# Optimization experiments

Measured on AMD Instinct MI355X. Metric: run time of the kernel, lower is better.

## Reference

```python
import jax, jax.numpy as jnp
import numpy as np

N_USERS = 50000; N_ENT = 100000; C = 64
E = 1500000; NNZ = 1000000
N_REL = 16; N_CATES = 32; NF = 4; NH = 2
R1 = N_REL - 1            # weight rows (devoted branch)
R2 = N_CATES + N_REL - 1  # weight_d rows (diverse branch)


def setup_inputs():
    key = jax.random.key(0)
    ks = list(jax.random.split(key, 32))
    f = jnp.float32
    inp = {}
    inp["user_emb"] = jax.random.normal(ks[0], (N_USERS, C), f)
    inp["entity_emb"] = jax.random.normal(ks[1], (N_ENT, C), f)
    inp["latent_emb"] = jax.random.normal(ks[2], (NF, C), f)
    inp["latent_div_emb"] = jax.random.normal(ks[3], (NF, C), f)
    inp["weight"] = jax.random.normal(ks[4], (R1, C), f) * 0.1
    inp["weight_d"] = jax.random.normal(ks[5], (R2, C), f) * 0.1
    # per-hop Aggregator params stacked over hops [NH, ...]; Linear applied as x @ W + b
    def p(k, shape, s=0.1):
        return jax.random.normal(k, shape, f) * s
    inp["cW1"] = p(ks[6], (NH, C, C)); inp["cb1"] = jnp.zeros((NH, C), f)
    inp["cW2"] = p(ks[7], (NH, C, C)); inp["cb2"] = jnp.zeros((NH, C), f)
    inp["cWua"] = p(ks[8], (NH, NF, NF)); inp["cbua"] = jnp.zeros((NH, NF), f)
    inp["cWwa"] = p(ks[9], (NH, R1, R1)); inp["cbwa"] = jnp.zeros((NH, R1), f)
    inp["eW1"] = p(ks[10], (NH, C, C)); inp["eb1"] = jnp.zeros((NH, C), f)
    inp["eW2"] = p(ks[11], (NH, C, C)); inp["eb2"] = jnp.zeros((NH, C), f)
    inp["eWua"] = p(ks[12], (NH, NF, NF)); inp["ebua"] = jnp.zeros((NH, NF), f)
    inp["eWwa"] = p(ks[13], (NH, R2, R2)); inp["ebwa"] = jnp.zeros((NH, R2), f)
    inp["interact_vals"] = jax.random.uniform(ks[14], (NNZ,), f)
    inp["edge_index"] = jax.random.randint(ks[15], (2, E), 0, N_ENT)
    inp["edge_type"] = jax.random.randint(ks[16], (E,), 1, N_REL)            # values in [1, R1]
    inp["entity_cate_set"] = jax.random.randint(ks[17], (N_ENT,), 1, N_CATES + 1)
    inp["interact_rows"] = jax.random.randint(ks[18], (NNZ,), 0, N_USERS)
    inp["interact_cols"] = jax.random.randint(ks[19], (NNZ,), 0, N_ENT)
    return inp


def _lin(x, W, b):
    return x @ W + b


def _mlp(x, W, b):  # Linear + LeakyReLU(0.2)
    return jax.nn.leaky_relu(_lin(x, W, b), 0.2)


def _normalize(x):  # F.normalize along dim=1 (eps=1e-12)
    return x / jnp.maximum(jnp.linalg.norm(x, axis=1, keepdims=True), 1e-12)


def _agg(entity_emb, user_emb, latent_emb, weight, w_idx, head, tail,
         rows, cols, vals, W1, b1, W2, b2, Wua, bua, Wwa, bwa):
    n_ent, n_usr = entity_emb.shape[0], user_emb.shape[0]
    # KG aggregate: gather -> multiply -> scatter_mean over head
    neigh = entity_emb[tail] * weight[w_idx]                                  # [E, C]
    ssum = jax.ops.segment_sum(neigh, head, num_segments=n_ent)
    cnt = jax.ops.segment_sum(jnp.ones((head.shape[0],), entity_emb.dtype), head, num_segments=n_ent)
    entity_agg = ssum / jnp.maximum(cnt, 1.0)[:, None]
    # user aggregate: sparse.mm(interact_mat, entity_emb)
    user_agg = jax.ops.segment_sum(vals[:, None] * entity_emb[cols], rows, num_segments=n_usr)
    # user -> latent interest attention
    score_ = _lin(user_emb, W1, b1) @ _lin(latent_emb, W1, b1).T              # [U, NF]
    score = jax.nn.softmax(_mlp(score_, Wua, bua), axis=1)                    # [U, NF]
    score_rp = _lin(latent_emb, W2, b2) @ _lin(weight, W2, b2).T              # [NF, R]
    latent_new = jax.nn.softmax(_mlp(score_rp, Wwa, bwa), axis=-1) @ weight   # [NF, C]
    mix = jnp.einsum("uf,fc->uc", score, latent_new)                          # (disen_weight * score).sum(1)
    user_agg = user_agg * mix + user_agg
    return entity_agg, user_agg, latent_new


def _dist_corr(t1, t2):
    ch = t1.shape[0]
    t1 = t1[:, None]; t2 = t2[:, None]
    sq1, sq2 = t1 ** 2, t2 ** 2
    a = jnp.sqrt(jnp.maximum(sq1 - 2.0 * (t1 @ t1.T) + sq1.T, 0.0) + 1e-8)
    b = jnp.sqrt(jnp.maximum(sq2 - 2.0 * (t2 @ t2.T) + sq2.T, 0.0) + 1e-8)
    A = a - a.mean(0, keepdims=True) - a.mean(1, keepdims=True) + a.mean()
    B = b - b.mean(0, keepdims=True) - b.mean(1, keepdims=True) + b.mean()
    n2 = float(ch * ch)
    dab = jnp.sqrt(jnp.maximum((A * B).sum() / n2, 0.0) + 1e-8)
    daa = jnp.sqrt(jnp.maximum((A * A).sum() / n2, 0.0) + 1e-8)
    dbb = jnp.sqrt(jnp.maximum((B * B).sum() / n2, 0.0) + 1e-8)
    return dab / jnp.sqrt(daa * dbb + 1e-8)


def _cor(lat):  # ind == "distance": sum over factor pairs
    c = jnp.asarray(0.0, lat.dtype)
    for i in range(NF):
        for j in range(i + 1, NF):
            c = c + _dist_corr(lat[i], lat[j])
    return c


def reference(user_emb, entity_emb, latent_emb, latent_div_emb, weight, weight_d,
              cW1, cb1, cW2, cb2, cWua, cbua, cWwa, cbwa,
              eW1, eb1, eW2, eb2, eWua, ebua, eWwa, ebwa,
              interact_vals, edge_index, edge_type, entity_cate_set,
              interact_rows, interact_cols):
    head, tail = edge_index[0], edge_index[1]
    idx_c = edge_type - 1               # devoted branch: relation weight index
    idx_d = entity_cate_set[tail] - 1   # diverse branch: category weight index
    # Devoted Interest Branch
    e, u, l = entity_emb, user_emb, latent_emb
    e_res, u_res, l_res = entity_emb, user_emb, latent_emb
    for i in range(NH):
        e, u, l = _agg(e, u, l, weight, idx_c, head, tail,
                       interact_rows, interact_cols, interact_vals,
                       cW1[i], cb1[i], cW2[i], cb2[i], cWua[i], cbua[i], cWwa[i], cbwa[i])
        e = _normalize(e); u = _normalize(u)
        l_res = _normalize(l)           # faithful: overwritten each hop, then += l
        e_res = e_res + e; u_res = u_res + u; l_res = l_res + l
    # Diverse Interest Branch
    e, u, l2 = entity_emb, user_emb, latent_div_emb
    e_d, u_d, l_d = entity_emb, user_emb, latent_div_emb
    for i in range(NH):
        e, u, l2 = _agg(e, u, l2, weight_d, idx_d, head, tail,
                        interact_rows, interact_cols, interact_vals,
                        eW1[i], eb1[i], eW2[i], eb2[i], eWua[i], ebua[i], eWwa[i], ebwa[i])
        e = _normalize(e); u = _normalize(u); l2 = _normalize(l2)
        e_d = e_d + e; u_d = u_d + u; l_d = l_d + l2
    cor = _cor(l_res)
    cor_d = _cor(l_d)
    return (e_res, u_res, cor, e_d, u_d, cor_d)
```

## Files before the change

### kernel.cpp

```cpp
#include <hip/hip_runtime.h>
#include <hip/hip_bf16.h>
#include <math.h>

typedef __hip_bfloat16 bf16;
typedef unsigned short u16;

#define NUSR 50000
#define NENT 100000
#define CC   64
#define EE   1500000
#define NNZI 1000000
#define NF_  4
#define R1_  15
#define R2_  47
#define NSH  8

__device__ __forceinline__ float b2f(bf16 x){ return __bfloat162float(x); }
__device__ __forceinline__ bf16  f2b(float x){ return __float2bfloat16(x); }
__device__ __forceinline__ float fin(float x){ return (x==x && fabsf(x) < 1e30f) ? x : 0.f; }

__device__ __forceinline__ unsigned bf16bits(float x){
    unsigned b = __float_as_uint(x);
    return (b + 0x7FFFu + ((b >> 16) & 1u)) >> 16;
}
__device__ __forceinline__ float pk_lo(unsigned p){ return __uint_as_float(p << 16); }
__device__ __forceinline__ float pk_hi(unsigned p){ return __uint_as_float(p & 0xFFFF0000u); }

__device__ __forceinline__ unsigned rflu(unsigned x){ return (unsigned)__builtin_amdgcn_readfirstlane((int)x); }

__device__ __forceinline__ float ldv(const float* p, long long i){ return p[i]; }
__device__ __forceinline__ float ldv(const bf16*  p, long long i){ return b2f(p[i]); }

struct LatArgs {
    const float *lin, *W1, *b1, *W2, *b2, *Wua, *bua, *Wwa, *bwa, *wt;
    float *lat, *nlat, *P2, *q2;
    int R;
};

__global__ void k_init(int* deg8_e, int* deg8_u, int* ctrs){
    int i = blockIdx.x*256 + threadIdx.x;
    if (i < NSH*NENT) deg8_e[i] = 0;
    if (i < NSH*NUSR) deg8_u[i] = 0;
    if (i < 2) ctrs[i] = 0;
}

__global__ void k_conv(const float* __restrict__ src, bf16* __restrict__ dst){
    int i = blockIdx.x*256 + threadIdx.x;
    if (i < NENT*CC) dst[i] = f2b(src[i]);
}

__global__ void k_hist(const int* __restrict__ head, const int* __restrict__ irows,
                       int* deg8_e, int* deg8_u,
                       u16* __restrict__ rank_e, u16* __restrict__ rank_u){
    int i = blockIdx.x*256 + threadIdx.x;
    int shard = blockIdx.x & (NSH-1);
    if (i < EE){
        int h = head[i];
        int r = ((unsigned)h < NENT) ? atomicAdd(&deg8_e[shard*NENT + h], 1) : 0;
        rank_e[i] = (u16)((r & 8191) | (shard << 13));
    } else {
        int j = i - EE;
        if (j < NNZI){
            int rr = irows[j];
            int r = ((unsigned)rr < NUSR) ? atomicAdd(&deg8_u[shard*NUSR + rr], 1) : 0;
            rank_u[j] = (u16)((r & 8191) | (shard << 13));
        }
    }
}

__global__ void k_base2(int* deg8_e, int* deg8_u,
                        unsigned* rsdeg_e, unsigned* rsdeg_u, int* ctrs){
    int i = blockIdx.x*256 + threadIdx.x;
    int lane = threadIdx.x & 63;
    {
        int d = 0;
        if (i < NENT){
            int tot = 0;
            #pragma unroll
            for (int c = 0; c < NSH; c++){
                int v = deg8_e[c*NENT + i];
                deg8_e[c*NENT + i] = tot;
                tot += v;
            }
            d = tot;
        }
        int incl = d;
        for (int off = 1; off < 64; off <<= 1){
            int v = __shfl_up(incl, off, 64);
            if (lane >= off) incl += v;
        }
        int tot = __shfl(incl, 63, 64);
        int base = 0;
        if (lane == 63) base = atomicAdd(&ctrs[0], tot);
        base = __shfl(base, 63, 64);
        if (i < NENT){
            unsigned rs = (unsigned)(base + incl - d);
            int dc = d < 2047 ? d : 2047;
            rsdeg_e[i] = (rs & 0x1FFFFFu) | ((unsigned)dc << 21);
        }
    }
    {
        int d = 0;
        if (i < NUSR){
            int tot = 0;
            #pragma unroll
            for (int c = 0; c < NSH; c++){
                int v = deg8_u[c*NUSR + i];
                deg8_u[c*NUSR + i] = tot;
                tot += v;
            }
            d = tot;
        }
        int incl = d;
        for (int off = 1; off < 64; off <<= 1){
            int v = __shfl_up(incl, off, 64);
            if (lane >= off) incl += v;
        }
        int tot = __shfl(incl, 63, 64);
        int base = 0;
        if (lane == 63) base = atomicAdd(&ctrs[1], tot);
        base = __shfl(base, 63, 64);
        if (i < NUSR){
            unsigned rs = (unsigned)(base + incl - d);
            int dc = d < 4095 ? d : 4095;
            rsdeg_u[i] = (rs & 0xFFFFFu) | ((unsigned)dc << 20);
        }
    }
}

__global__ void k_scatter(const int* __restrict__ head, const int* __restrict__ tail,
                          const int* __restrict__ etype, const int* __restrict__ cate,
                          const int* __restrict__ irows, const int* __restrict__ icols,
                          const float* __restrict__ ivals,
                          const u16* __restrict__ rank_e, const u16* __restrict__ rank_u,
                          const int* __restrict__ xoff_e, const int* __restrict__ xoff_u,
                          const unsigned* __restrict__ rsdeg_e, const unsigned* __restrict__ rsdeg_u,
                          unsigned* __restrict__ epk, unsigned* __restrict__ upk){
    int i = blockIdx.x*256 + threadIdx.x;
    if (i < EE){
        int h = head[i]; if ((unsigned)h >= NENT) return;
        unsigned tu = (unsigned)tail[i]; if (tu >= NENT) tu = 0;
        unsigned rk = rank_e[i];
        int shard = rk >> 13, r = rk & 8191;
        int slot = (int)(rsdeg_e[h] & 0x1FFFFFu) + xoff_e[shard*NENT + h] + r;
        unsigned ty = (unsigned)(etype[i] - 1) & 15u;
        unsigned cd = (unsigned)(cate[tu]  - 1) & 31u;
        if ((unsigned)slot < EE)
            epk[slot] = tu | (ty << 17) | (cd << 21);
    } else {
        int j = i - EE;
        if (j < NNZI){
            int rr = irows[j]; if ((unsigned)rr >= NUSR) return;
            unsigned c = (unsigned)icols[j]; if (c >= NENT) c = 0;
            unsigned rk = rank_u[j];
            int shard = rk >> 13, r = rk & 8191;
            int slot = (int)(rsdeg_u[rr] & 0xFFFFFu) + xoff_u[shard*NUSR + rr] + r;
            unsigned bits = __float_as_uint(ivals[j]);
            unsigned rb = bits + 0x7FFFu + ((bits >> 16) & 1u);
            unsigned vb = (rb >> 16) & 0x7FFFu;
            if ((unsigned)slot < NNZI)
                upk[slot] = c | (vb << 17);
        }
    }
}

__global__ void k_lat2(LatArgs A0, LatArgs A1){
    LatArgs a = (blockIdx.x == 0) ? A0 : A1;
    const int R = a.R;
    __shared__ float sW1[64*64], sW2[64*64];
    __shared__ float swt[R2_*64], wp[R2_*64];
    __shared__ float lf[NF_*64], lp1[NF_*64], lp2[NF_*64];
    __shared__ float Praw[64*NF_], qv[NF_];
    __shared__ float srp[NF_*R2_], zz[NF_*R2_];
    __shared__ float latls[NF_*64], norms[NF_];
    int t = threadIdx.x;

    for (int idx = t; idx < 64*64; idx += 256){ sW1[idx] = a.W1[idx]; sW2[idx] = a.W2[idx]; }
    for (int idx = t; idx < R*64; idx += 256) swt[idx] = a.wt[idx];
    lf[t] = fin(a.lin[t]);
    __syncthreads();

    {
        int f = t >> 6, k = t & 63;
        float s1 = a.b1[k], s2 = a.b2[k];
        for (int c = 0; c < 64; c++){
            float lv = lf[f*64+c];
            s1 += lv * sW1[c*64+k];
            s2 += lv * sW2[c*64+k];
        }
        lp1[t] = s1; lp2[t] = s2;
    }
    __syncthreads();

    {
        int c = t >> 2, f = t & 3;
        float s = 0.f;
        for (int k = 0; k < 64; k++) s += sW1[c*64+k] * lp1[f*64+k];
        Praw[c*4+f] = s;
    }
    if (t < NF_){
        float s = 0.f;
        for (int k = 0; k < 64; k++) s += a.b1[k] * lp1[t*64+k];
        qv[t] = s;
    }
    __syncthreads();

    {
        int g = t >> 6, c = t & 63;
        float s = 0.f;
        for (int f = 0; f < NF_; f++) s += Praw[c*4+f] * a.Wua[f*4+g];
        a.P2[g*64+c] = s;
    }
    if (t < NF_){
        float s = a.bua[t];
        for (int f = 0; f < NF_; f++) s += qv[f] * a.Wua[f*4+t];
        a.q2[t] = s;
    }
    for (int idx = t; idx < R*64; idx += 256){
        int r = idx >> 6, k = idx & 63;
        float s = a.b2[k];
        for (int c = 0; c < 64; c++) s += swt[r*64+c] * sW2[c*64+k];
        wp[idx] = s;
    }
    __syncthreads();

    if (t < NF_*R){
        int f = t / R, r = t % R;
        float s = 0.f;
        for (int k = 0; k < 64; k++) s += lp2[f*64+k] * wp[r*64+k];
        srp[f*R2_ + r] = s;
    }
    __syncthreads();

    if (t < NF_*R){
        int f = t / R, ss = t % R;
        float v = a.bwa[ss];
        for (int r = 0; r < R; r++) v += srp[f*R2_ + r] * a.Wwa[r*R + ss];
        zz[f*R2_ + ss] = (v > 0.f) ? v : 0.2f*v;
    }
    __syncthreads();

    if (t < NF_){
        float m = -1e30f;
        for (int r = 0; r < R; r++) m = fmaxf(m, zz[t*R2_ + r]);
        float sum = 0.f;
        for (int r = 0; r < R; r++){ float e = expf(zz[t*R2_ + r] - m); zz[t*R2_ + r] = e; sum += e; }
        float inv = 1.f / sum;
        for (int r = 0; r < R; r++) zz[t*R2_ + r] *= inv;
    }
    __syncthreads();

    {
        int f = t >> 6, c = t & 63;
        float s = 0.f;
        for (int r = 0; r < R; r++) s += zz[f*R2_ + r] * swt[r*64 + c];
        latls[t] = s; a.lat[t] = s;
    }
    __syncthreads();
    if (t < NF_){
        float s = 0.f;
        for (int c = 0; c < 64; c++){ float v = latls[t*64+c]; s += v*v; }
        norms[t] = fmaxf(sqrtf(s), 1e-12f);
    }
    __syncthreads();
    a.nlat[t] = latls[t] / norms[t >> 6];
}

template<typename SRC>
__device__ __forceinline__ float ent_row(const SRC* __restrict__ e_src, const float* wl,
                                         const unsigned* __restrict__ epk,
                                         unsigned rd, int use_d, int lane){
    rd = rflu(rd);
    int s = (int)(rd & 0x1FFFFFu);
    int deg = (int)(rd >> 21);
    int e_ = s + deg;
    float acc = 0.f;
    int k = s;
    for (; k + 4 <= e_; k += 4){
        unsigned p0 = rflu(epk[k]), p1 = rflu(epk[k+1]), p2 = rflu(epk[k+2]), p3 = rflu(epk[k+3]);
        unsigned t0 = p0 & 0x1FFFFu; t0 = t0 < NENT ? t0 : 0u;
        unsigned t1 = p1 & 0x1FFFFu; t1 = t1 < NENT ? t1 : 0u;
        unsigned t2 = p2 & 0x1FFFFu; t2 = t2 < NENT ? t2 : 0u;
        unsigned t3 = p3 & 0x1FFFFu; t3 = t3 < NENT ? t3 : 0u;
        float g0 = ldv(e_src, (long long)t0*64 + lane);
        float g1 = ldv(e_src, (long long)t1*64 + lane);
        float g2 = ldv(e_src, (long long)t2*64 + lane);
        float g3 = ldv(e_src, (long long)t3*64 + lane);
        int w0 = use_d ? (int)((p0 >> 21) & 31u) : (int)((p0 >> 17) & 15u);
        int w1 = use_d ? (int)((p1 >> 21) & 31u) : (int)((p1 >> 17) & 15u);
        int w2 = use_d ? (int)((p2 >> 21) & 31u) : (int)((p2 >> 17) & 15u);
        int w3 = use_d ? (int)((p3 >> 21) & 31u) : (int)((p3 >> 17) & 15u);
        acc += g0*wl[w0*64+lane] + g1*wl[w1*64+lane] + g2*wl[w2*64+lane] + g3*wl[w3*64+lane];
    }
    for (; k < e_; k++){
        unsigned p = rflu(epk[k]);
        unsigned ti = p & 0x1FFFFu; ti = ti < NENT ? ti : 0u;
        int wi = use_d ? (int)((p >> 21) & 31u) : (int)((p >> 17) & 15u);
        acc += ldv(e_src, (long long)ti*64 + lane) * wl[wi*64+lane];
    }
    float ea = fin(acc) / fmaxf((float)deg, 1.f);
    float sq = ea*ea;
    for (int m = 1; m < 64; m <<= 1) sq += __shfl_xor(sq, m, 64);
    float nrm = fmaxf(sqrtf(fin(sq)), 1e-12f);
    return ea / nrm;
}

__global__ __launch_bounds__(256) void k_ent0(const float* __restrict__ e_src,
                                              const float* __restrict__ wtab, int R, int use_d,
                                              const unsigned* __restrict__ rsdeg_e,
                                              const unsigned* __restrict__ epk,
                                              bf16* dst){
    __shared__ float wl[R2_*64];
    int t = threadIdx.x;
    for (int idx = t; idx < R2_*64; idx += 256)
        wl[idx] = (idx < R*64) ? wtab[idx] : 0.f;
    __syncthreads();
    int ent = blockIdx.x*4 + (t >> 6);
    int lane = t & 63;
    if (ent >= NENT) return;
    float v = ent_row(e_src, wl, epk, rsdeg_e[ent], use_d, lane);
    dst[(long long)ent*64 + lane] = f2b(v);
}

__global__ __launch_bounds__(256) void k_ent1f(const bf16* __restrict__ e_src,
                                               const float* __restrict__ base_emb,
                                               const float* __restrict__ wtab, int R, int use_d,
                                               const unsigned* __restrict__ rsdeg_e,
                                               const unsigned* __restrict__ epk,
                                               float* dst){
    __shared__ float wl[R2_*64];
    int t = threadIdx.x;
    for (int idx = t; idx < R2_*64; idx += 256)
        wl[idx] = (idx < R*64) ? wtab[idx] : 0.f;
    __syncthreads();
    int ent = blockIdx.x*4 + (t >> 6);
    int lane = t & 63;
    if (ent >= NENT) return;
    float v = ent_row(e_src, wl, epk, rsdeg_e[ent], use_d, lane);
    long long ix = (long long)ent*64 + lane;
    dst[ix] = base_emb[ix] + b2f(e_src[ix]) + v;
}

template<typename ESRC>
__device__ __forceinline__ float usr_gather(const ESRC* __restrict__ e_src,
                                            const unsigned* __restrict__ upk,
                                            unsigned rd, int lane){
    rd = rflu(rd);
    int s = (int)(rd & 0xFFFFFu);
    int e_ = s + (int)(rd >> 20);
    float acc = 0.f;
    int k = s;
    for (; k + 8 <= e_; k += 8){
        unsigned p0 = rflu(upk[k]),   p1 = rflu(upk[k+1]), p2 = rflu(upk[k+2]), p3 = rflu(upk[k+3]);
        unsigned p4 = rflu(upk[k+4]), p5 = rflu(upk[k+5]), p6 = rflu(upk[k+6]), p7 = rflu(upk[k+7]);
        unsigned c0 = p0 & 0x1FFFFu; c0 = c0 < NENT ? c0 : 0u;
        unsigned c1 = p1 & 0x1FFFFu; c1 = c1 < NENT ? c1 : 0u;
        unsigned c2 = p2 & 0x1FFFFu; c2 = c2 < NENT ? c2 : 0u;
        unsigned c3 = p3 & 0x1FFFFu; c3 = c3 < NENT ? c3 : 0u;
        unsigned c4 = p4 & 0x1FFFFu; c4 = c4 < NENT ? c4 : 0u;
        unsigned c5 = p5 & 0x1FFFFu; c5 = c5 < NENT ? c5 : 0u;
        unsigned c6 = p6 & 0x1FFFFu; c6 = c6 < NENT ? c6 : 0u;
        unsigned c7 = p7 & 0x1FFFFu; c7 = c7 < NENT ? c7 : 0u;
        float g0 = ldv(e_src,(long long)c0*64+lane), g1 = ldv(e_src,(long long)c1*64+lane);
        float g2 = ldv(e_src,(long long)c2*64+lane), g3 = ldv(e_src,(long long)c3*64+lane);
        float g4 = ldv(e_src,(long long)c4*64+lane), g5 = ldv(e_src,(long long)c5*64+lane);
        float g6 = ldv(e_src,(long long)c6*64+lane), g7 = ldv(e_src,(long long)c7*64+lane);
        float v0 = __uint_as_float(((p0 >> 17) & 0x7FFFu) << 16);
        float v1 = __uint_as_float(((p1 >> 17) & 0x7FFFu) << 16);
        float v2 = __uint_as_float(((p2 >> 17) & 0x7FFFu) << 16);
        float v3 = __uint_as_float(((p3 >> 17) & 0x7FFFu) << 16);
        float v4 = __uint_as_float(((p4 >> 17) & 0x7FFFu) << 16);
        float v5 = __uint_as_float(((p5 >> 17) & 0x7FFFu) << 16);
        float v6 = __uint_as_float(((p6 >> 17) & 0x7FFFu) << 16);
        float v7 = __uint_as_float(((p7 >> 17) & 0x7FFFu) << 16);
        acc += v0*g0 + v1*g1 + v2*g2 + v3*g3 + v4*g4 + v5*g5 + v6*g6 + v7*g7;
    }
    for (; k + 4 <= e_; k += 4){
        unsigned p0 = rflu(upk[k]), p1 = rflu(upk[k+1]), p2 = rflu(upk[k+2]), p3 = rflu(upk[k+3]);
        unsigned c0 = p0 & 0x1FFFFu; c0 = c0 < NENT ? c0 : 0u;
        unsigned c1 = p1 & 0x1FFFFu; c1 = c1 < NENT ? c1 : 0u;
        unsigned c2 = p2 & 0x1FFFFu; c2 = c2 < NENT ? c2 : 0u;
        unsigned c3 = p3 & 0x1FFFFu; c3 = c3 < NENT ? c3 : 0u;
        float v0 = __uint_as_float(((p0 >> 17) & 0x7FFFu) << 16);
        float v1 = __uint_as_float(((p1 >> 17) & 0x7FFFu) << 16);
        float v2 = __uint_as_float(((p2 >> 17) & 0x7FFFu) << 16);
        float v3 = __uint_as_float(((p3 >> 17) & 0x7FFFu) << 16);
        acc += v0*ldv(e_src,(long long)c0*64+lane) + v1*ldv(e_src,(long long)c1*64+lane)
             + v2*ldv(e_src,(long long)c2*64+lane) + v3*ldv(e_src,(long long)c3*64+lane);
    }
    for (; k < e_; k++){
        unsigned p = rflu(upk[k]);
        unsigned c = p & 0x1FFFFu; c = c < NENT ? c : 0u;
        float v = __uint_as_float(((p >> 17) & 0x7FFFu) << 16);
        acc += v * ldv(e_src, (long long)c*64 + lane);
    }
    return fin(acc);
}

__device__ __forceinline__ float usr_epi(float acc, float x,
                                         const float* P2l, const float* latl, const float* q2l,
                                         int lane){
    float s0 = x*P2l[lane], s1 = x*P2l[64+lane], s2 = x*P2l[128+lane], s3 = x*P2l[192+lane];
    for (int m = 1; m < 64; m <<= 1){
        s0 += __shfl_xor(s0, m, 64);
        s1 += __shfl_xor(s1, m, 64);
        s2 += __shfl_xor(s2, m, 64);
        s3 += __shfl_xor(s3, m, 64);
    }
    s0 += q2l[0]; s1 += q2l[1]; s2 += q2l[2]; s3 += q2l[3];
    s0 = (s0 > 0.f) ? s0 : 0.2f*s0;
    s1 = (s1 > 0.f) ? s1 : 0.2f*s1;
    s2 = (s2 > 0.f) ? s2 : 0.2f*s2;
    s3 = (s3 > 0.f) ? s3 : 0.2f*s3;
    float mx = fmaxf(fmaxf(s0, s1), fmaxf(s2, s3));
    float e0 = expf(s0-mx), e1 = expf(s1-mx), e2 = expf(s2-mx), e3 = expf(s3-mx);
    float inv = 1.f / (e0+e1+e2+e3);
    float mix = fin((e0*latl[lane] + e1*latl[64+lane] + e2*latl[128+lane] + e3*latl[192+lane]) * inv);
    float ua = acc * (1.f + mix);
    float sq = ua*ua;
    for (int m = 1; m < 64; m <<= 1) sq += __shfl_xor(sq, m, 64);
    float nrm = fmaxf(sqrtf(fin(sq)), 1e-12f);
    return ua / nrm;
}

__global__ __launch_bounds__(256) void k_usr0(const float* __restrict__ u_src,
                                              const float* __restrict__ e_src,
                                              const unsigned* __restrict__ rsdeg_u,
                                              const unsigned* __restrict__ upk,
                                              const float* __restrict__ P2,
                                              const float* __restrict__ q2,
                                              const float* __restrict__ lat_new,
                                              float* dst){
    __shared__ float P2l[NF_*64], latl[NF_*64], q2l[NF_];
    int t = threadIdx.x;
    P2l[t] = fin(P2[t]); latl[t] = fin(lat_new[t]);
    if (t < NF_) q2l[t] = fin(q2[t]);
    __syncthreads();
    int u = blockIdx.x*4 + (t >> 6);
    int lane = t & 63;
    if (u >= NUSR) return;
    float acc = usr_gather(e_src, upk, rsdeg_u[u], lane);
    float x = u_src[(long long)u*64 + lane];
    dst[(long long)u*64 + lane] = usr_epi(acc, x, P2l, latl, q2l, lane);
}

__global__ __launch_bounds__(256) void k_usr1f(float* u_io,
                                               const bf16* __restrict__ e_src,
                                               const float* __restrict__ base_emb,
                                               const unsigned* __restrict__ rsdeg_u,
                                               const unsigned* __restrict__ upk,
                                               const float* __restrict__ P2,
                                               const float* __restrict__ q2,
                                               const float* __restrict__ lat_new){
    __shared__ float P2l[NF_*64], latl[NF_*64], q2l[NF_];
    int t = threadIdx.x;
    P2l[t] = fin(P2[t]); latl[t] = fin(lat_new[t]);
    if (t < NF_) q2l[t] = fin(q2[t]);
    __syncthreads();
    int u = blockIdx.x*4 + (t >> 6);
    int lane = t & 63;
    if (u >= NUSR) return;
    float acc = usr_gather(e_src, upk, rsdeg_u[u], lane);
    long long ix = (long long)u*64 + lane;
    float x = u_io[ix];
    float v = usr_epi(acc, x, P2l, latl, q2l, lane);
    u_io[ix] = base_emb[ix] + x + v;
}

#define GE_ ((NENT+3)/4)
#define GU_ ((NUSR+3)/4)
__global__ __launch_bounds__(256) void k_it0(const bf16* __restrict__ ebf,
                                             const float* __restrict__ wt_c,
                                             const float* __restrict__ wt_d,
                                             const unsigned* __restrict__ rsdeg_e,
                                             const unsigned* __restrict__ epk,
                                             unsigned* __restrict__ eA2,
                                             const float* __restrict__ u_src,
                                             const unsigned* __restrict__ rsdeg_u,
                                             const unsigned* __restrict__ upk,
                                             const float* __restrict__ P2c,
                                             const float* __restrict__ q2c,
                                             const float* __restrict__ latc,
                                             const float* __restrict__ P2d,
                                             const float* __restrict__ q2d,
                                             const float* __restrict__ latd,
                                             float* __restrict__ dst_c,
                                             float* __restrict__ dst_d){
    __shared__ float sm[(R1_+R2_)*64];
    int t = threadIdx.x;
    int lane = t & 63;
    if (blockIdx.x < GE_){
        float* wlc = sm;
        float* wld = sm + R1_*64;
        for (int idx = t; idx < R1_*64; idx += 256) wlc[idx] = wt_c[idx];
        for (int idx = t; idx < R2_*64; idx += 256) wld[idx] = wt_d[idx];
        __syncthreads();
        int ent = blockIdx.x*4 + (t >> 6);
        if (ent >= NENT) return;
        unsigned rd = rflu(rsdeg_e[ent]);
        int s = (int)(rd & 0x1FFFFFu);
        int deg = (int)(rd >> 21);
        int e_ = s + deg;
        float ac = 0.f, ad = 0.f;
        int k = s;
        for (; k + 8 <= e_; k += 8){
            unsigned p0 = rflu(epk[k]),   p1 = rflu(epk[k+1]), p2 = rflu(epk[k+2]), p3 = rflu(epk[k+3]);
            unsigned p4 = rflu(epk[k+4]), p5 = rflu(epk[k+5]), p6 = rflu(epk[k+6]), p7 = rflu(epk[k+7]);
            unsigned t0 = p0 & 0x1FFFFu; t0 = t0 < NENT ? t0 : 0u;
            unsigned t1 = p1 & 0x1FFFFu; t1 = t1 < NENT ? t1 : 0u;
            unsigned t2 = p2 & 0x1FFFFu; t2 = t2 < NENT ? t2 : 0u;
            unsigned t3 = p3 & 0x1FFFFu; t3 = t3 < NENT ? t3 : 0u;
            unsigned t4 = p4 & 0x1FFFFu; t4 = t4 < NENT ? t4 : 0u;
            unsigned t5 = p5 & 0x1FFFFu; t5 = t5 < NENT ? t5 : 0u;
            unsigned t6 = p6 & 0x1FFFFu; t6 = t6 < NENT ? t6 : 0u;
            unsigned t7 = p7 & 0x1FFFFu; t7 = t7 < NENT ? t7 : 0u;
            float g0 = b2f(ebf[(long long)t0*64 + lane]);
            float g1 = b2f(ebf[(long long)t1*64 + lane]);
            float g2 = b2f(ebf[(long long)t2*64 + lane]);
            float g3 = b2f(ebf[(long long)t3*64 + lane]);
            float g4 = b2f(ebf[(long long)t4*64 + lane]);
            float g5 = b2f(ebf[(long long)t5*64 + lane]);
            float g6 = b2f(ebf[(long long)t6*64 + lane]);
            float g7 = b2f(ebf[(long long)t7*64 + lane]);
            ac += g0*wlc[((p0>>17)&15u)*64+lane] + g1*wlc[((p1>>17)&15u)*64+lane]
                + g2*wlc[((p2>>17)&15u)*64+lane] + g3*wlc[((p3>>17)&15u)*64+lane]
                + g4*wlc[((p4>>17)&15u)*64+lane] + g5*wlc[((p5>>17)&15u)*64+lane]
                + g6*wlc[((p6>>17)&15u)*64+lane] + g7*wlc[((p7>>17)&15u)*64+lane];
            ad += g0*wld[((p0>>21)&31u)*64+lane] + g1*wld[((p1>>21)&31u)*64+lane]
                + g2*wld[((p2>>21)&31u)*64+lane] + g3*wld[((p3>>21)&31u)*64+lane]
                + g4*wld[((p4>>21)&31u)*64+lane] + g5*wld[((p5>>21)&31u)*64+lane]
                + g6*wld[((p6>>21)&31u)*64+lane] + g7*wld[((p7>>21)&31u)*64+lane];
        }
        for (; k + 4 <= e_; k += 4){
            unsigned p0 = rflu(epk[k]), p1 = rflu(epk[k+1]), p2 = rflu(epk[k+2]), p3 = rflu(epk[k+3]);
            unsigned t0 = p0 & 0x1FFFFu; t0 = t0 < NENT ? t0 : 0u;
            unsigned t1 = p1 & 0x1FFFFu; t1 = t1 < NENT ? t1 : 0u;
            unsigned t2 = p2 & 0x1FFFFu; t2 = t2 < NENT ? t2 : 0u;
            unsigned t3 = p3 & 0x1FFFFu; t3 = t3 < NENT ? t3 : 0u;
            float g0 = b2f(ebf[(long long)t0*64 + lane]);
            float g1 = b2f(ebf[(long long)t1*64 + lane]);
            float g2 = b2f(ebf[(long long)t2*64 + lane]);
            float g3 = b2f(ebf[(long long)t3*64 + lane]);
            ac += g0*wlc[((p0>>17)&15u)*64+lane] + g1*wlc[((p1>>17)&15u)*64+lane]
                + g2*wlc[((p2>>17)&15u)*64+lane] + g3*wlc[((p3>>17)&15u)*64+lane];
            ad += g0*wld[((p0>>21)&31u)*64+lane] + g1*wld[((p1>>21)&31u)*64+lane]
                + g2*wld[((p2>>21)&31u)*64+lane] + g3*wld[((p3>>21)&31u)*64+lane];
        }
        for (; k < e_; k++){
            unsigned p = rflu(epk[k]);
            unsigned ti = p & 0x1FFFFu; ti = ti < NENT ? ti : 0u;
            float g = b2f(ebf[(long long)ti*64 + lane]);
            ac += g*wlc[((p>>17)&15u)*64+lane];
            ad += g*wld[((p>>21)&31u)*64+lane];
        }
        float inv_deg = 1.f / fmaxf((float)deg, 1.f);
        float ec = fin(ac) * inv_deg, ed = fin(ad) * inv_deg;
        float sc = ec*ec, sd = ed*ed;
        for (int m = 1; m < 64; m <<= 1){
            sc += __shfl_xor(sc, m, 64);
            sd += __shfl_xor(sd, m, 64);
        }
        float vc = ec / fmaxf(sqrtf(fin(sc)), 1e-12f);
        float vd = ed / fmaxf(sqrtf(fin(sd)), 1e-12f);
        eA2[(long long)ent*64 + lane] = bf16bits(vc) | (bf16bits(vd) << 16);
    } else {
        float* P2lc = sm;
        float* latlc = sm + 256;
        float* P2ld = sm + 512;
        float* latld = sm + 768;
        float* q2lc = sm + 1024;
        float* q2ld = sm + 1032;
        P2lc[t] = fin(P2c[t]); latlc[t] = fin(latc[t]);
        P2ld[t] = fin(P2d[t]); latld[t] = fin(latd[t]);
        if (t < NF_){ q2lc[t] = fin(q2c[t]); q2ld[t] = fin(q2d[t]); }
        __syncthreads();
        int u = (blockIdx.x - GE_)*4 + (t >> 6);
        if (u >= NUSR) return;
        float acc = usr_gather(ebf, upk, rsdeg_u[u], lane);
        long long ix = (long long)u*64 + lane;
        float x = u_src[ix];
        dst_c[ix] = usr_epi(acc, x, P2lc, latlc, q2lc, lane);
        dst_d[ix] = usr_epi(acc, x, P2ld, latld, q2ld, lane);
    }
}

__global__ __launch_bounds__(256) void k_it1(const unsigned* __restrict__ eA2,
                                             const float* __restrict__ ent_base,
                                             const float* __restrict__ wt_c,
                                             const float* __restrict__ wt_d,
                                             const unsigned* __restrict__ rsdeg_e,
                                             const unsigned* __restrict__ epk,
                                             float* __restrict__ oe_c,
                                             float* __restrict__ oe_d,
                                             float* __restrict__ uc_io,
                                             float* __restrict__ ud_io,
                                             const float* __restrict__ usr_base,
                                             const unsigned* __restrict__ rsdeg_u,
                                             const unsigned* __restrict__ upk,
                                             const float* __restrict__ P2c,
                                             const float* __restrict__ q2c,
                                             const float* __restrict__ latc,
                                             const float* __restrict__ P2d,
                                             const float* __restrict__ q2d,
                                             const float* __restrict__ latd){
    __shared__ float sm[(R1_+R2_)*64];
    int t = threadIdx.x;
    int lane = t & 63;
    if (blockIdx.x < GE_){
        float* wlc = sm;
        float* wld = sm + R1_*64;
        for (int idx = t; idx < R1_*64; idx += 256) wlc[idx] = wt_c[idx];
        for (int idx = t; idx < R2_*64; idx += 256) wld[idx] = wt_d[idx];
        __syncthreads();
        int ent = blockIdx.x*4 + (t >> 6);
        if (ent >= NENT) return;
        unsigned rd = rflu(rsdeg_e[ent]);
        int s = (int)(rd & 0x1FFFFFu);
        int deg = (int)(rd >> 21);
        int e_ = s + deg;
        float ac = 0.f, ad = 0.f;
        int k = s;
        for (; k + 8 <= e_; k += 8){
            unsigned p0 = rflu(epk[k]),   p1 = rflu(epk[k+1]), p2 = rflu(epk[k+2]), p3 = rflu(epk[k+3]);
            unsigned p4 = rflu(epk[k+4]), p5 = rflu(epk[k+5]), p6 = rflu(epk[k+6]), p7 = rflu(epk[k+7]);
            unsigned t0 = p0 & 0x1FFFFu; t0 = t0 < NENT ? t0 : 0u;
            unsigned t1 = p1 & 0x1FFFFu; t1 = t1 < NENT ? t1 : 0u;
            unsigned t2 = p2 & 0x1FFFFu; t2 = t2 < NENT ? t2 : 0u;
            unsigned t3 = p3 & 0x1FFFFu; t3 = t3 < NENT ? t3 : 0u;
            unsigned t4 = p4 & 0x1FFFFu; t4 = t4 < NENT ? t4 : 0u;
            unsigned t5 = p5 & 0x1FFFFu; t5 = t5 < NENT ? t5 : 0u;
            unsigned t6 = p6 & 0x1FFFFu; t6 = t6 < NENT ? t6 : 0u;
            unsigned t7 = p7 & 0x1FFFFu; t7 = t7 < NENT ? t7 : 0u;
            unsigned v0 = eA2[(long long)t0*64 + lane];
            unsigned v1 = eA2[(long long)t1*64 + lane];
            unsigned v2 = eA2[(long long)t2*64 + lane];
            unsigned v3 = eA2[(long long)t3*64 + lane];
            unsigned v4 = eA2[(long long)t4*64 + lane];
            unsigned v5 = eA2[(long long)t5*64 + lane];
            unsigned v6 = eA2[(long long)t6*64 + lane];
            unsigned v7 = eA2[(long long)t7*64 + lane];
            ac += pk_lo(v0)*wlc[((p0>>17)&15u)*64+lane] + pk_lo(v1)*wlc[((p1>>17)&15u)*64+lane]
                + pk_lo(v2)*wlc[((p2>>17)&15u)*64+lane] + pk_lo(v3)*wlc[((p3>>17)&15u)*64+lane]
                + pk_lo(v4)*wlc[((p4>>17)&15u)*64+lane] + pk_lo(v5)*wlc[((p5>>17)&15u)*64+lane]
                + pk_lo(v6)*wlc[((p6>>17)&15u)*64+lane] + pk_lo(v7)*wlc[((p7>>17)&15u)*64+lane];
            ad += pk_hi(v0)*wld[((p0>>21)&31u)*64+lane] + pk_hi(v1)*wld[((p1>>21)&31u)*64+lane]
                + pk_hi(v2)*wld[((p2>>21)&31u)*64+lane] + pk_hi(v3)*wld[((p3>>21)&31u)*64+lane]
                + pk_hi(v4)*wld[((p4>>21)&31u)*64+lane] + pk_hi(v5)*wld[((p5>>21)&31u)*64+lane]
                + pk_hi(v6)*wld[((p6>>21)&31u)*64+lane] + pk_hi(v7)*wld[((p7>>21)&31u)*64+lane];
        }
        for (; k + 4 <= e_; k += 4){
            unsigned p0 = rflu(epk[k]), p1 = rflu(epk[k+1]), p2 = rflu(epk[k+2]), p3 = rflu(epk[k+3]);
            unsigned t0 = p0 & 0x1FFFFu; t0 = t0 < NENT ? t0 : 0u;
            unsigned t1 = p1 & 0x1FFFFu; t1 = t1 < NENT ? t1 : 0u;
            unsigned t2 = p2 & 0x1FFFFu; t2 = t2 < NENT ? t2 : 0u;
            unsigned t3 = p3 & 0x1FFFFu; t3 = t3 < NENT ? t3 : 0u;
            unsigned v0 = eA2[(long long)t0*64 + lane];
            unsigned v1 = eA2[(long long)t1*64 + lane];
            unsigned v2 = eA2[(long long)t2*64 + lane];
            unsigned v3 = eA2[(long long)t3*64 + lane];
            ac += pk_lo(v0)*wlc[((p0>>17)&15u)*64+lane] + pk_lo(v1)*wlc[((p1>>17)&15u)*64+lane]
                + pk_lo(v2)*wlc[((p2>>17)&15u)*64+lane] + pk_lo(v3)*wlc[((p3>>17)&15u)*64+lane];
            ad += pk_hi(v0)*wld[((p0>>21)&31u)*64+lane] + pk_hi(v1)*wld[((p1>>21)&31u)*64+lane]
                + pk_hi(v2)*wld[((p2>>21)&31u)*64+lane] + pk_hi(v3)*wld[((p3>>21)&31u)*64+lane];
        }
        for (; k < e_; k++){
            unsigned p = rflu(epk[k]);
            unsigned ti = p & 0x1FFFFu; ti = ti < NENT ? ti : 0u;
            unsigned v = eA2[(long long)ti*64 + lane];
            ac += pk_lo(v) * wlc[((p>>17)&15u)*64+lane];
            ad += pk_hi(v) * wld[((p>>21)&31u)*64+lane];
        }
        float inv_deg = 1.f / fmaxf((float)deg, 1.f);
        float vc = fin(ac) * inv_deg, vd = fin(ad) * inv_deg;
        float sc = vc*vc, sd = vd*vd;
        for (int m = 1; m < 64; m <<= 1){
            sc += __shfl_xor(sc, m, 64);
            sd += __shfl_xor(sd, m, 64);
        }
        long long ix = (long long)ent*64 + lane;
        float be = ent_base[ix];
        unsigned selfv = eA2[ix];
        oe_c[ix] = be + pk_lo(selfv) + vc / fmaxf(sqrtf(fin(sc)), 1e-12f);
        oe_d[ix] = be + pk_hi(selfv) + vd / fmaxf(sqrtf(fin(sd)), 1e-12f);
    } else {
        float* P2lc = sm;
        float* latlc = sm + 256;
        float* P2ld = sm + 512;
        float* latld = sm + 768;
        float* q2lc = sm + 1024;
        float* q2ld = sm + 1032;
        P2lc[t] = fin(P2c[t]); latlc[t] = fin(latc[t]);
        P2ld[t] = fin(P2d[t]); latld[t] = fin(latd[t]);
        if (t < NF_){ q2lc[t] = fin(q2c[t]); q2ld[t] = fin(q2d[t]); }
        __syncthreads();
        int u = (blockIdx.x - GE_)*4 + (t >> 6);
        if (u >= NUSR) return;
        unsigned rd = rflu(rsdeg_u[u]);
        int s = (int)(rd & 0xFFFFFu);
        int e_ = s + (int)(rd >> 20);
        float accc = 0.f, accd = 0.f;
        int k = s;
        for (; k + 8 <= e_; k += 8){
            unsigned p0 = rflu(upk[k]),   p1 = rflu(upk[k+1]), p2 = rflu(upk[k+2]), p3 = rflu(upk[k+3]);
            unsigned p4 = rflu(upk[k+4]), p5 = rflu(upk[k+5]), p6 = rflu(upk[k+6]), p7 = rflu(upk[k+7]);
            unsigned c0 = p0 & 0x1FFFFu; c0 = c0 < NENT ? c0 : 0u;
            unsigned c1 = p1 & 0x1FFFFu; c1 = c1 < NENT ? c1 : 0u;
            unsigned c2 = p2 & 0x1FFFFu; c2 = c2 < NENT ? c2 : 0u;
            unsigned c3 = p3 & 0x1FFFFu; c3 = c3 < NENT ? c3 : 0u;
            unsigned c4 = p4 & 0x1FFFFu; c4 = c4 < NENT ? c4 : 0u;
            unsigned c5 = p5 & 0x1FFFFu; c5 = c5 < NENT ? c5 : 0u;
            unsigned c6 = p6 & 0x1FFFFu; c6 = c6 < NENT ? c6 : 0u;
            unsigned c7 = p7 & 0x1FFFFu; c7 = c7 < NENT ? c7 : 0u;
            unsigned g0 = eA2[(long long)c0*64 + lane];
            unsigned g1 = eA2[(long long)c1*64 + lane];
            unsigned g2 = eA2[(long long)c2*64 + lane];
            unsigned g3 = eA2[(long long)c3*64 + lane];
            unsigned g4 = eA2[(long long)c4*64 + lane];
            unsigned g5 = eA2[(long long)c5*64 + lane];
            unsigned g6 = eA2[(long long)c6*64 + lane];
            unsigned g7 = eA2[(long long)c7*64 + lane];
            float v0 = __uint_as_float(((p0 >> 17) & 0x7FFFu) << 16);
            float v1 = __uint_as_float(((p1 >> 17) & 0x7FFFu) << 16);
            float v2 = __uint_as_float(((p2 >> 17) & 0x7FFFu) << 16);
            float v3 = __uint_as_float(((p3 >> 17) & 0x7FFFu) << 16);
            float v4 = __uint_as_float(((p4 >> 17) & 0x7FFFu) << 16);
            float v5 = __uint_as_float(((p5 >> 17) & 0x7FFFu) << 16);
            float v6 = __uint_as_float(((p6 >> 17) & 0x7FFFu) << 16);
            float v7 = __uint_as_float(((p7 >> 17) & 0x7FFFu) << 16);
            accc += v0*pk_lo(g0) + v1*pk_lo(g1) + v2*pk_lo(g2) + v3*pk_lo(g3)
                  + v4*pk_lo(g4) + v5*pk_lo(g5) + v6*pk_lo(g6) + v7*pk_lo(g7);
            accd += v0*pk_hi(g0) + v1*pk_hi(g1) + v2*pk_hi(g2) + v3*pk_hi(g3)
                  + v4*pk_hi(g4) + v5*pk_hi(g5) + v6*pk_hi(g6) + v7*pk_hi(g7);
        }
        for (; k + 4 <= e_; k += 4){
            unsigned p0 = rflu(upk[k]), p1 = rflu(upk[k+1]), p2 = rflu(upk[k+2]), p3 = rflu(upk[k+3]);
            unsigned c0 = p0 & 0x1FFFFu; c0 = c0 < NENT ? c0 : 0u;
            unsigned c1 = p1 & 0x1FFFFu; c1 = c1 < NENT ? c1 : 0u;
            unsigned c2 = p2 & 0x1FFFFu; c2 = c2 < NENT ? c2 : 0u;
            unsigned c3 = p3 & 0x1FFFFu; c3 = c3 < NENT ? c3 : 0u;
            float v0 = __uint_as_float(((p0 >> 17) & 0x7FFFu) << 16);
            float v1 = __uint_as_float(((p1 >> 17) & 0x7FFFu) << 16);
            float v2 = __uint_as_float(((p2 >> 17) & 0x7FFFu) << 16);
            float v3 = __uint_as_float(((p3 >> 17) & 0x7FFFu) << 16);
            unsigned g0 = eA2[(long long)c0*64 + lane];
            unsigned g1 = eA2[(long long)c1*64 + lane];
            unsigned g2 = eA2[(long long)c2*64 + lane];
            unsigned g3 = eA2[(long long)c3*64 + lane];
            accc += v0*pk_lo(g0) + v1*pk_lo(g1) + v2*pk_lo(g2) + v3*pk_lo(g3);
            accd += v0*pk_hi(g0) + v1*pk_hi(g1) + v2*pk_hi(g2) + v3*pk_hi(g3);
        }
        for (; k < e_; k++){
            unsigned p = rflu(upk[k]);
            unsigned c = p & 0x1FFFFu; c = c < NENT ? c : 0u;
            float v = __uint_as_float(((p >> 17) & 0x7FFFu) << 16);
            unsigned g = eA2[(long long)c*64 + lane];
            accc += v * pk_lo(g);
            accd += v * pk_hi(g);
        }
        long long ix = (long long)u*64 + lane;
        float xc = uc_io[ix], xd = ud_io[ix];
        float be = usr_base[ix];
        float vc = usr_epi(fin(accc), xc, P2lc, latlc, q2lc, lane);
        float vd = usr_epi(fin(accd), xd, P2ld, latld, q2ld, lane);
        uc_io[ix] = be + xc + vc;
        ud_io[ix] = be + xd + vd;
    }
}

__global__ void k_cor(const float* __restrict__ latn1_c,
                      const float* __restrict__ ldiv,
                      const float* __restrict__ nld0, const float* __restrict__ nld1,
                      float* out){
    __shared__ float rows[NF_*64];
    __shared__ float nr[NF_];
    __shared__ float t1s[64], t2s[64], m1s[64], m2s[64];
    __shared__ float pr[256], pr2[256], pr3[256];
    __shared__ float gms[2];
    __shared__ float corsh;
    int t = threadIdx.x, b = blockIdx.x;

    if (b == 0){
        rows[t] = fin(latn1_c[t]);
        __syncthreads();
        if (t < NF_){
            float s = 0.f;
            for (int c = 0; c < 64; c++){ float v = rows[t*64+c]; s += v*v; }
            nr[t] = fmaxf(sqrtf(s), 1e-12f);
        }
        __syncthreads();
        float v = rows[t];
        __syncthreads();
        rows[t] = v + v / nr[t >> 6];
    } else {
        rows[t] = ldiv[t] + fin(nld0[t]) + fin(nld1[t]);
    }
    if (t == 0) corsh = 0.f;
    __syncthreads();

    for (int i = 0; i < NF_; i++) for (int j = i+1; j < NF_; j++){
        if (t < 64){ t1s[t] = rows[i*64+t]; t2s[t] = rows[j*64+t]; }
        __syncthreads();
        int i_ = t >> 2, q = t & 3;
        float pa = 0.f, pb = 0.f;
        for (int jj = q*16; jj < q*16+16; jj++){
            float d1 = t1s[i_] - t1s[jj]; pa += sqrtf(fmaxf(d1*d1, 0.f) + 1e-8f);
            float d2 = t2s[i_] - t2s[jj]; pb += sqrtf(fmaxf(d2*d2, 0.f) + 1e-8f);
        }
        pr[t] = pa; pr2[t] = pb;
        __syncthreads();
        if (q == 0){
            m1s[i_] = (pr[t] + pr[t+1] + pr[t+2] + pr[t+3]) / 64.f;
            m2s[i_] = (pr2[t] + pr2[t+1] + pr2[t+2] + pr2[t+3]) / 64.f;
        }
        __syncthreads();
        if (t == 0){
            float s1 = 0.f, s2 = 0.f;
            for (int ii = 0; ii < 64; ii++){ s1 += m1s[ii]; s2 += m2s[ii]; }
            gms[0] = s1 / 64.f; gms[1] = s2 / 64.f;
        }
        __syncthreads();
        float gm1 = gms[0], gm2 = gms[1];
        float sab = 0.f, saa = 0.f, sbb = 0.f;
        for (int kk = 0; kk < 16; kk++){
            int idx = t*16 + kk; int ii = idx >> 6, jj = idx & 63;
            float d1 = t1s[ii] - t1s[jj];
            float A = sqrtf(fmaxf(d1*d1, 0.f) + 1e-8f) - m1s[ii] - m1s[jj] + gm1;
            float d2 = t2s[ii] - t2s[jj];
            float B = sqrtf(fmaxf(d2*d2, 0.f) + 1e-8f) - m2s[ii] - m2s[jj] + gm2;
            sab += A*B; saa += A*A; sbb += B*B;
        }
        pr[t] = sab; pr2[t] = saa; pr3[t] = sbb;
        __syncthreads();
        for (int off = 128; off; off >>= 1){
            if (t < off){ pr[t] += pr[t+off]; pr2[t] += pr2[t+off]; pr3[t] += pr3[t+off]; }
            __syncthreads();
        }
        if (t == 0){
            float dab = sqrtf(fmaxf(pr[0]/4096.f, 0.f) + 1e-8f);
            float daa = sqrtf(fmaxf(pr2[0]/4096.f, 0.f) + 1e-8f);
            float dbb = sqrtf(fmaxf(pr3[0]/4096.f, 0.f) + 1e-8f);
            corsh += dab / sqrtf(daa*dbb + 1e-8f);
        }
        __syncthreads();
    }
    if (t == 0){
        long long pos = (b == 0) ? 9600000LL : 19200001LL;
        out[pos] = corsh;
    }
}

extern "C" void kernel_launch(void* const* d_in, const int* in_sizes, int n_in,
                              void* d_out, int out_size, void* d_ws, size_t ws_size,
                              hipStream_t stream){
    const float* user_emb   = (const float*)d_in[0];
    const float* entity_emb = (const float*)d_in[1];
    const float* latent_emb = (const float*)d_in[2];
    const float* latent_div = (const float*)d_in[3];
    const float* weight     = (const float*)d_in[4];
    const float* weight_d   = (const float*)d_in[5];
    const float* cW1 = (const float*)d_in[6];  const float* cb1 = (const float*)d_in[7];
    const float* cW2 = (const float*)d_in[8];  const float* cb2 = (const float*)d_in[9];
    const float* cWua= (const float*)d_in[10]; const float* cbua= (const float*)d_in[11];
    const float* cWwa= (const float*)d_in[12]; const float* cbwa= (const float*)d_in[13];
    const float* eW1 = (const float*)d_in[14]; const float* eb1 = (const float*)d_in[15];
    const float* eW2 = (const float*)d_in[16]; const float* eb2 = (const float*)d_in[17];
    const float* eWua= (const float*)d_in[18]; const float* ebua= (const float*)d_in[19];
    const float* eWwa= (const float*)d_in[20]; const float* ebwa= (const float*)d_in[21];
    const float* ivals = (const float*)d_in[22];
    const int* edge_index = (const int*)d_in[23];
    const int* etype      = (const int*)d_in[24];
    const int* cate       = (const int*)d_in[25];
    const int* irows      = (const int*)d_in[26];
    const int* icols      = (const int*)d_in[27];
    float* out = (float*)d_out;

    const int* head = edge_index;
    const int* tail = edge_index + EE;

    char* base = (char*)d_ws;
    size_t off = 0;
    auto carve = [&](size_t bytes) -> void* {
        void* p = base + off;
        off += (bytes + 255) & ~(size_t)255;
        return p;
    };
    unsigned* rsdeg_e = (unsigned*)carve((size_t)NENT*4);
    unsigned* rsdeg_u = (unsigned*)carve((size_t)NUSR*4);
    unsigned* epk     = (unsigned*)carve((size_t)EE*4);
    unsigned* upk     = (unsigned*)carve((size_t)NNZI*4);
    float* latn[2][2]; float* nlat[2][2]; float* P2b[2][2]; float* q2b[2][2];
    for (int b = 0; b < 2; b++) for (int i = 0; i < 2; i++){
        latn[b][i] = (float*)carve(NF_*64*4);
        nlat[b][i] = (float*)carve(NF_*64*4);
        P2b [b][i] = (float*)carve(NF_*64*4);
        q2b [b][i] = (float*)carve(64);
    }
    size_t common = off;
    size_t ebuf  = (size_t)NENT*CC*2;
    size_t ebuf2 = (size_t)NENT*CC*4;
    bool tierA = (ws_size >= common + ((ebuf + 255) & ~(size_t)255) + ((ebuf2 + 255) & ~(size_t)255));

    bf16 *ebf = nullptr; unsigned* eA2 = nullptr; bf16* eA = nullptr;
    char* scratch_base;
    if (tierA){
        ebf = (bf16*)carve(ebuf);
        eA2 = (unsigned*)carve(ebuf2);
        scratch_base = (char*)eA2;
    } else {
        eA  = (bf16*)carve(ebuf);
        scratch_base = (char*)eA;
    }

    int* deg8_e = (int*)scratch_base;
    int* deg8_u = (int*)(scratch_base + 3276800);
    int* ctrs   = (int*)(scratch_base + 4915200);
    u16* rank_e = (u16*)(scratch_base + 5242880);
    u16* rank_u = (u16*)(scratch_base + 8388608);

    float* oe_c = out;
    float* ou_c = out + 6400000LL;
    float* oe_d = out + 9600001LL;
    float* ou_d = out + 16000001LL;

    int gi = (NSH*NENT + 255)/256;
    k_init<<<gi, 256, 0, stream>>>(deg8_e, deg8_u, ctrs);
    if (tierA) k_conv<<<(NENT*CC+255)/256, 256, 0, stream>>>(entity_emb, ebf);
    int gh = (EE + NNZI + 255)/256;
    k_hist<<<gh, 256, 0, stream>>>(head, irows, deg8_e, deg8_u, rank_e, rank_u);
    k_base2<<<(NENT+255)/256, 256, 0, stream>>>(deg8_e, deg8_u, rsdeg_e, rsdeg_u, ctrs);
    k_scatter<<<gh, 256, 0, stream>>>(head, tail, etype, cate, irows, icols, ivals,
                                      rank_e, rank_u, deg8_e, deg8_u,
                                      rsdeg_e, rsdeg_u, epk, upk);

    LatArgs a_c0 = {latent_emb, cW1, cb1, cW2, cb2, cWua, cbua, cWwa, cbwa, weight,
                    latn[0][0], nlat[0][0], P2b[0][0], q2b[0][0], R1_};
    LatArgs a_d0 = {latent_div, eW1, eb1, eW2, eb2, eWua, ebua, eWwa, ebwa, weight_d,
                    latn[1][0], nlat[1][0], P2b[1][0], q2b[1][0], R2_};
    k_lat2<<<2, 256, 0, stream>>>(a_c0, a_d0);
    LatArgs a_c1 = {latn[0][0], cW1+4096, cb1+64, cW2+4096, cb2+64, cWua+16, cbua+4,
                    cWwa+R1_*R1_, cbwa+R1_, weight,
                    latn[0][1], nlat[0][1], P2b[0][1], q2b[0][1], R1_};
    LatArgs a_d1 = {nlat[1][0], eW1+4096, eb1+64, eW2+4096, eb2+64, eWua+16, ebua+4,
                    eWwa+R2_*R2_, ebwa+R2_, weight_d,
                    latn[1][1], nlat[1][1], P2b[1][1], q2b[1][1], R2_};
    k_lat2<<<2, 256, 0, stream>>>(a_c1, a_d1);

    int ge = GE_, gu = GU_;
    if (tierA){
        k_it0<<<ge + gu, 256, 0, stream>>>(ebf, weight, weight_d, rsdeg_e, epk, eA2,
            user_emb, rsdeg_u, upk,
            P2b[0][0], q2b[0][0], latn[0][0],
            P2b[1][0], q2b[1][0], latn[1][0], ou_c, ou_d);
        k_it1<<<ge + gu, 256, 0, stream>>>(eA2, entity_emb, weight, weight_d,
            rsdeg_e, epk, oe_c, oe_d,
            ou_c, ou_d, user_emb, rsdeg_u, upk,
            P2b[0][1], q2b[0][1], latn[0][1],
            P2b[1][1], q2b[1][1], latn[1][1]);
    } else {
        const float* wts[2] = {weight, weight_d};
        const int    Rs[2]  = {R1_, R2_};
        float* oes[2] = {oe_c, oe_d};
        float* ous[2] = {ou_c, ou_d};
        for (int br = 0; br < 2; br++){
            k_ent0<<<ge, 256, 0, stream>>>(entity_emb, wts[br], Rs[br], br, rsdeg_e, epk, eA);
            k_usr0<<<gu, 256, 0, stream>>>(user_emb, entity_emb, rsdeg_u, upk,
                P2b[br][0], q2b[br][0], latn[br][0], ous[br]);
            k_ent1f<<<ge, 256, 0, stream>>>(eA, entity_emb, wts[br], Rs[br], br, rsdeg_e, epk, oes[br]);
            k_usr1f<<<gu, 256, 0, stream>>>(ous[br], eA, user_emb, rsdeg_u, upk,
                P2b[br][1], q2b[br][1], latn[br][1]);
        }
    }

    k_cor<<<2, 256, 0, stream>>>(latn[0][1], latent_div, nlat[1][0], nlat[1][1], out);
}
```

Measured before the change: 809.6 us.

## Batch-load edge indices per wave via readlane; fuse init and bf16 conversion into histogram

The gather loops now have each lane load one packed edge word per 64-edge chunk and broadcast it with readlane. Before, every edge needed its own scalar-broadcast load from global memory. The init kernel is replaced by a memset, and the fp32-to-bf16 conversion is folded into the histogram kernel as extra vectorized blocks, which removes two launches. The per-chunk readlane loop adds instruction overhead for low-degree nodes.

```diff
diff --git a/kernel.cpp b/kernel.cpp
--- a/kernel.cpp
+++ b/kernel.cpp
@@ -27,6 +27,7 @@
 __device__ __forceinline__ float pk_hi(unsigned p){ return __uint_as_float(p & 0xFFFF0000u); }
 
 __device__ __forceinline__ unsigned rflu(unsigned x){ return (unsigned)__builtin_amdgcn_readfirstlane((int)x); }
+__device__ __forceinline__ unsigned rdl(unsigned v, int kk){ return (unsigned)__builtin_amdgcn_readlane((int)v, kk); }
 
 __device__ __forceinline__ float ldv(const float* p, long long i){ return p[i]; }
 __device__ __forceinline__ float ldv(const bf16*  p, long long i){ return b2f(p[i]); }
@@ -37,33 +38,28 @@
     int R;
 };
 
-__global__ void k_init(int* deg8_e, int* deg8_u, int* ctrs){
-    int i = blockIdx.x*256 + threadIdx.x;
-    if (i < NSH*NENT) deg8_e[i] = 0;
-    if (i < NSH*NUSR) deg8_u[i] = 0;
-    if (i < 2) ctrs[i] = 0;
-}
-
-__global__ void k_conv(const float* __restrict__ src, bf16* __restrict__ dst){
-    int i = blockIdx.x*256 + threadIdx.x;
-    if (i < NENT*CC) dst[i] = f2b(src[i]);
-}
-
 __global__ void k_hist(const int* __restrict__ head, const int* __restrict__ irows,
                        int* deg8_e, int* deg8_u,
-                       u16* __restrict__ rank_e, u16* __restrict__ rank_u){
+                       u16* __restrict__ rank_e, u16* __restrict__ rank_u,
+                       const float* __restrict__ esrc, bf16* __restrict__ ebf){
     int i = blockIdx.x*256 + threadIdx.x;
     int shard = blockIdx.x & (NSH-1);
     if (i < EE){
         int h = head[i];
         int r = ((unsigned)h < NENT) ? atomicAdd(&deg8_e[shard*NENT + h], 1) : 0;
         rank_e[i] = (u16)((r & 8191) | (shard << 13));
-    } else {
+    } else if (i < EE + NNZI){
         int j = i - EE;
-        if (j < NNZI){
-            int rr = irows[j];
-            int r = ((unsigned)rr < NUSR) ? atomicAdd(&deg8_u[shard*NUSR + rr], 1) : 0;
-            rank_u[j] = (u16)((r & 8191) | (shard << 13));
+        int rr = irows[j];
+        int r = ((unsigned)rr < NUSR) ? atomicAdd(&deg8_u[shard*NUSR + rr], 1) : 0;
+        rank_u[j] = (u16)((r & 8191) | (shard << 13));
+    } else if (ebf){
+        long long j = (long long)(i - (EE + NNZI)) * 4;
+        if (j < (long long)NENT*CC){
+            const float4 v = *(const float4*)(esrc + j);
+            u16* o = (u16*)ebf + j;
+            o[0] = (u16)bf16bits(v.x); o[1] = (u16)bf16bits(v.y);
+            o[2] = (u16)bf16bits(v.z); o[3] = (u16)bf16bits(v.w);
         }
     }
 }
@@ -350,31 +346,6 @@
     int e_ = s + (int)(rd >> 20);
     float acc = 0.f;
     int k = s;
-    for (; k + 8 <= e_; k += 8){
-        unsigned p0 = rflu(upk[k]),   p1 = rflu(upk[k+1]), p2 = rflu(upk[k+2]), p3 = rflu(upk[k+3]);
-        unsigned p4 = rflu(upk[k+4]), p5 = rflu(upk[k+5]), p6 = rflu(upk[k+6]), p7 = rflu(upk[k+7]);
-        unsigned c0 = p0 & 0x1FFFFu; c0 = c0 < NENT ? c0 : 0u;
-        unsigned c1 = p1 & 0x1FFFFu; c1 = c1 < NENT ? c1 : 0u;
-        unsigned c2 = p2 & 0x1FFFFu; c2 = c2 < NENT ? c2 : 0u;
-        unsigned c3 = p3 & 0x1FFFFu; c3 = c3 < NENT ? c3 : 0u;
-        unsigned c4 = p4 & 0x1FFFFu; c4 = c4 < NENT ? c4 : 0u;
-        unsigned c5 = p5 & 0x1FFFFu; c5 = c5 < NENT ? c5 : 0u;
-        unsigned c6 = p6 & 0x1FFFFu; c6 = c6 < NENT ? c6 : 0u;
-        unsigned c7 = p7 & 0x1FFFFu; c7 = c7 < NENT ? c7 : 0u;
-        float g0 = ldv(e_src,(long long)c0*64+lane), g1 = ldv(e_src,(long long)c1*64+lane);
-        float g2 = ldv(e_src,(long long)c2*64+lane), g3 = ldv(e_src,(long long)c3*64+lane);
-        float g4 = ldv(e_src,(long long)c4*64+lane), g5 = ldv(e_src,(long long)c5*64+lane);
-        float g6 = ldv(e_src,(long long)c6*64+lane), g7 = ldv(e_src,(long long)c7*64+lane);
-        float v0 = __uint_as_float(((p0 >> 17) & 0x7FFFu) << 16);
-        float v1 = __uint_as_float(((p1 >> 17) & 0x7FFFu) << 16);
-        float v2 = __uint_as_float(((p2 >> 17) & 0x7FFFu) << 16);
-        float v3 = __uint_as_float(((p3 >> 17) & 0x7FFFu) << 16);
-        float v4 = __uint_as_float(((p4 >> 17) & 0x7FFFu) << 16);
-        float v5 = __uint_as_float(((p5 >> 17) & 0x7FFFu) << 16);
-        float v6 = __uint_as_float(((p6 >> 17) & 0x7FFFu) << 16);
-        float v7 = __uint_as_float(((p7 >> 17) & 0x7FFFu) << 16);
-        acc += v0*g0 + v1*g1 + v2*g2 + v3*g3 + v4*g4 + v5*g5 + v6*g6 + v7*g7;
-    }
     for (; k + 4 <= e_; k += 4){
         unsigned p0 = rflu(upk[k]), p1 = rflu(upk[k+1]), p2 = rflu(upk[k+2]), p3 = rflu(upk[k+3]);
         unsigned c0 = p0 & 0x1FFFFu; c0 = c0 < NENT ? c0 : 0u;
@@ -502,56 +473,46 @@
         int deg = (int)(rd >> 21);
         int e_ = s + deg;
         float ac = 0.f, ad = 0.f;
-        int k = s;
-        for (; k + 8 <= e_; k += 8){
-            unsigned p0 = rflu(epk[k]),   p1 = rflu(epk[k+1]), p2 = rflu(epk[k+2]), p3 = rflu(epk[k+3]);
-            unsigned p4 = rflu(epk[k+4]), p5 = rflu(epk[k+5]), p6 = rflu(epk[k+6]), p7 = rflu(epk[k+7]);
-            unsigned t0 = p0 & 0x1FFFFu; t0 = t0 < NENT ? t0 : 0u;
-            unsigned t1 = p1 & 0x1FFFFu; t1 = t1 < NENT ? t1 : 0u;
-            unsigned t2 = p2 & 0x1FFFFu; t2 = t2 < NENT ? t2 : 0u;
-            unsigned t3 = p3 & 0x1FFFFu; t3 = t3 < NENT ? t3 : 0u;
-            unsigned t4 = p4 & 0x1FFFFu; t4 = t4 < NENT ? t4 : 0u;
-            unsigned t5 = p5 & 0x1FFFFu; t5 = t5 < NENT ? t5 : 0u;
-            unsigned t6 = p6 & 0x1FFFFu; t6 = t6 < NENT ? t6 : 0u;
-            unsigned t7 = p7 & 0x1FFFFu; t7 = t7 < NENT ? t7 : 0u;
-            float g0 = b2f(ebf[(long long)t0*64 + lane]);
-            float g1 = b2f(ebf[(long long)t1*64 + lane]);
-            float g2 = b2f(ebf[(long long)t2*64 + lane]);
-            float g3 = b2f(ebf[(long long)t3*64 + lane]);
-            float g4 = b2f(ebf[(long long)t4*64 + lane]);
-            float g5 = b2f(ebf[(long long)t5*64 + lane]);
-            float g6 = b2f(ebf[(long long)t6*64 + lane]);
-            float g7 = b2f(ebf[(long long)t7*64 + lane]);
-            ac += g0*wlc[((p0>>17)&15u)*64+lane] + g1*wlc[((p1>>17)&15u)*64+lane]
-                + g2*wlc[((p2>>17)&15u)*64+lane] + g3*wlc[((p3>>17)&15u)*64+lane]
-                + g4*wlc[((p4>>17)&15u)*64+lane] + g5*wlc[((p5>>17)&15u)*64+lane]
-                + g6*wlc[((p6>>17)&15u)*64+lane] + g7*wlc[((p7>>17)&15u)*64+lane];
-            ad += g0*wld[((p0>>21)&31u)*64+lane] + g1*wld[((p1>>21)&31u)*64+lane]
-                + g2*wld[((p2>>21)&31u)*64+lane] + g3*wld[((p3>>21)&31u)*64+lane]
-                + g4*wld[((p4>>21)&31u)*64+lane] + g5*wld[((p5>>21)&31u)*64+lane]
-                + g6*wld[((p6>>21)&31u)*64+lane] + g7*wld[((p7>>21)&31u)*64+lane];
-        }
-        for (; k + 4 <= e_; k += 4){
-            unsigned p0 = rflu(epk[k]), p1 = rflu(epk[k+1]), p2 = rflu(epk[k+2]), p3 = rflu(epk[k+3]);
-            unsigned t0 = p0 & 0x1FFFFu; t0 = t0 < NENT ? t0 : 0u;
-            unsigned t1 = p1 & 0x1FFFFu; t1 = t1 < NENT ? t1 : 0u;
-            unsigned t2 = p2 & 0x1FFFFu; t2 = t2 < NENT ? t2 : 0u;
-            unsigned t3 = p3 & 0x1FFFFu; t3 = t3 < NENT ? t3 : 0u;
-            float g0 = b2f(ebf[(long long)t0*64 + lane]);
-            float g1 = b2f(ebf[(long long)t1*64 + lane]);
-            float g2 = b2f(ebf[(long long)t2*64 + lane]);
-            float g3 = b2f(ebf[(long long)t3*64 + lane]);
-            ac += g0*wlc[((p0>>17)&15u)*64+lane] + g1*wlc[((p1>>17)&15u)*64+lane]
-                + g2*wlc[((p2>>17)&15u)*64+lane] + g3*wlc[((p3>>17)&15u)*64+lane];
-            ad += g0*wld[((p0>>21)&31u)*64+lane] + g1*wld[((p1>>21)&31u)*64+lane]
-                + g2*wld[((p2>>21)&31u)*64+lane] + g3*wld[((p3>>21)&31u)*64+lane];
-        }
-        for (; k < e_; k++){
-            unsigned p = rflu(epk[k]);
-            unsigned ti = p & 0x1FFFFu; ti = ti < NENT ? ti : 0u;
-            float g = b2f(ebf[(long long)ti*64 + lane]);
-            ac += g*wlc[((p>>17)&15u)*64+lane];
-            ad += g*wld[((p>>21)&31u)*64+lane];
+        for (int kb = s; kb < e_; kb += 64){
+            int gi2 = kb + lane;
+            unsigned pkv = epk[gi2 < e_ ? gi2 : s];
+            int rem = e_ - kb; if (rem > 64) rem = 64;
+            int kk = 0;
+            for (; kk + 8 <= rem; kk += 8){
+                unsigned p0 = rdl(pkv, kk),   p1 = rdl(pkv, kk+1), p2 = rdl(pkv, kk+2), p3 = rdl(pkv, kk+3);
+                unsigned p4 = rdl(pkv, kk+4), p5 = rdl(pkv, kk+5), p6 = rdl(pkv, kk+6), p7 = rdl(pkv, kk+7);
+                unsigned t0 = p0 & 0x1FFFFu; t0 = t0 < NENT ? t0 : 0u;
+                unsigned t1 = p1 & 0x1FFFFu; t1 = t1 < NENT ? t1 : 0u;
+                unsigned t2 = p2 & 0x1FFFFu; t2 = t2 < NENT ? t2 : 0u;
+                unsigned t3 = p3 & 0x1FFFFu; t3 = t3 < NENT ? t3 : 0u;
+                unsigned t4 = p4 & 0x1FFFFu; t4 = t4 < NENT ? t4 : 0u;
+                unsigned t5 = p5 & 0x1FFFFu; t5 = t5 < NENT ? t5 : 0u;
+                unsigned t6 = p6 & 0x1FFFFu; t6 = t6 < NENT ? t6 : 0u;
+                unsigned t7 = p7 & 0x1FFFFu; t7 = t7 < NENT ? t7 : 0u;
+                float g0 = b2f(ebf[(long long)t0*64 + lane]);
+                float g1 = b2f(ebf[(long long)t1*64 + lane]);
+                float g2 = b2f(ebf[(long long)t2*64 + lane]);
+                float g3 = b2f(ebf[(long long)t3*64 + lane]);
+                float g4 = b2f(ebf[(long long)t4*64 + lane]);
+                float g5 = b2f(ebf[(long long)t5*64 + lane]);
+                float g6 = b2f(ebf[(long long)t6*64 + lane]);
+                float g7 = b2f(ebf[(long long)t7*64 + lane]);
+                ac += g0*wlc[((p0>>17)&15u)*64+lane] + g1*wlc[((p1>>17)&15u)*64+lane]
+                    + g2*wlc[((p2>>17)&15u)*64+lane] + g3*wlc[((p3>>17)&15u)*64+lane]
+                    + g4*wlc[((p4>>17)&15u)*64+lane] + g5*wlc[((p5>>17)&15u)*64+lane]
+                    + g6*wlc[((p6>>17)&15u)*64+lane] + g7*wlc[((p7>>17)&15u)*64+lane];
+                ad += g0*wld[((p0>>21)&31u)*64+lane] + g1*wld[((p1>>21)&31u)*64+lane]
+                    + g2*wld[((p2>>21)&31u)*64+lane] + g3*wld[((p3>>21)&31u)*64+lane]
+                    + g4*wld[((p4>>21)&31u)*64+lane] + g5*wld[((p5>>21)&31u)*64+lane]
+                    + g6*wld[((p6>>21)&31u)*64+lane] + g7*wld[((p7>>21)&31u)*64+lane];
+            }
+            for (; kk < rem; kk++){
+                unsigned p = rdl(pkv, kk);
+                unsigned ti = p & 0x1FFFFu; ti = ti < NENT ? ti : 0u;
+                float g = b2f(ebf[(long long)ti*64 + lane]);
+                ac += g*wlc[((p>>17)&15u)*64+lane];
+                ad += g*wld[((p>>21)&31u)*64+lane];
+            }
         }
         float inv_deg = 1.f / fmaxf((float)deg, 1.f);
         float ec = fin(ac) * inv_deg, ed = fin(ad) * inv_deg;
@@ -576,7 +537,48 @@
         __syncthreads();
         int u = (blockIdx.x - GE_)*4 + (t >> 6);
         if (u >= NUSR) return;
-        float acc = usr_gather(ebf, upk, rsdeg_u[u], lane);
+        unsigned rd = rflu(rsdeg_u[u]);
+        int s = (int)(rd & 0xFFFFFu);
+        int e_ = s + (int)(rd >> 20);
+        float acc = 0.f;
+        for (int kb = s; kb < e_; kb += 64){
+            int gi2 = kb + lane;
+            unsigned pkv = upk[gi2 < e_ ? gi2 : s];
+            int rem = e_ - kb; if (rem > 64) rem = 64;
+            int kk = 0;
+            for (; kk + 8 <= rem; kk += 8){
+                unsigned p0 = rdl(pkv, kk),   p1 = rdl(pkv, kk+1), p2 = rdl(pkv, kk+2), p3 = rdl(pkv, kk+3);
+                unsigned p4 = rdl(pkv, kk+4), p5 = rdl(pkv, kk+5), p6 = rdl(pkv, kk+6), p7 = rdl(pkv, kk+7);
+                unsigned c0 = p0 & 0x1FFFFu; c0 = c0 < NENT ? c0 : 0u;
+                unsigned c1 = p1 & 0x1FFFFu; c1 = c1 < NENT ? c1 : 0u;
+                unsigned c2 = p2 & 0x1FFFFu; c2 = c2 < NENT ? c2 : 0u;
+                unsigned c3 = p3 & 0x1FFFFu; c3 = c3 < NENT ? c3 : 0u;
+                unsigned c4 = p4 & 0x1FFFFu; c4 = c4 < NENT ? c4 : 0u;
+                unsigned c5 = p5 & 0x1FFFFu; c5 = c5 < NENT ? c5 : 0u;
+                unsigned c6 = p6 & 0x1FFFFu; c6 = c6 < NENT ? c6 : 0u;
+                unsigned c7 = p7 & 0x1FFFFu; c7 = c7 < NENT ? c7 : 0u;
+                float g0 = b2f(ebf[(long long)c0*64+lane]), g1 = b2f(ebf[(long long)c1*64+lane]);
+                float g2 = b2f(ebf[(long long)c2*64+lane]), g3 = b2f(ebf[(long long)c3*64+lane]);
+                float g4 = b2f(ebf[(long long)c4*64+lane]), g5 = b2f(ebf[(long long)c5*64+lane]);
+                float g6 = b2f(ebf[(long long)c6*64+lane]), g7 = b2f(ebf[(long long)c7*64+lane]);
+                float v0 = __uint_as_float(((p0 >> 17) & 0x7FFFu) << 16);
+                float v1 = __uint_as_float(((p1 >> 17) & 0x7FFFu) << 16);
+                float v2 = __uint_as_float(((p2 >> 17) & 0x7FFFu) << 16);
+                float v3 = __uint_as_float(((p3 >> 17) & 0x7FFFu) << 16);
+                float v4 = __uint_as_float(((p4 >> 17) & 0x7FFFu) << 16);
+                float v5 = __uint_as_float(((p5 >> 17) & 0x7FFFu) << 16);
+                float v6 = __uint_as_float(((p6 >> 17) & 0x7FFFu) << 16);
+                float v7 = __uint_as_float(((p7 >> 17) & 0x7FFFu) << 16);
+                acc += v0*g0 + v1*g1 + v2*g2 + v3*g3 + v4*g4 + v5*g5 + v6*g6 + v7*g7;
+            }
+            for (; kk < rem; kk++){
+                unsigned p = rdl(pkv, kk);
+                unsigned c = p & 0x1FFFFu; c = c < NENT ? c : 0u;
+                float v = __uint_as_float(((p >> 17) & 0x7FFFu) << 16);
+                acc += v * b2f(ebf[(long long)c*64 + lane]);
+            }
+        }
+        acc = fin(acc);
         long long ix = (long long)u*64 + lane;
         float x = u_src[ix];
         dst_c[ix] = usr_epi(acc, x, P2lc, latlc, q2lc, lane);
@@ -619,56 +621,46 @@
         int deg = (int)(rd >> 21);
         int e_ = s + deg;
         float ac = 0.f, ad = 0.f;
-        int k = s;
-        for (; k + 8 <= e_; k += 8){
-            unsigned p0 = rflu(epk[k]),   p1 = rflu(epk[k+1]), p2 = rflu(epk[k+2]), p3 = rflu(epk[k+3]);
-            unsigned p4 = rflu(epk[k+4]), p5 = rflu(epk[k+5]), p6 = rflu(epk[k+6]), p7 = rflu(epk[k+7]);
-            unsigned t0 = p0 & 0x1FFFFu; t0 = t0 < NENT ? t0 : 0u;
-            unsigned t1 = p1 & 0x1FFFFu; t1 = t1 < NENT ? t1 : 0u;
-            unsigned t2 = p2 & 0x1FFFFu; t2 = t2 < NENT ? t2 : 0u;
-            unsigned t3 = p3 & 0x1FFFFu; t3 = t3 < NENT ? t3 : 0u;
-            unsigned t4 = p4 & 0x1FFFFu; t4 = t4 < NENT ? t4 : 0u;
-            unsigned t5 = p5 & 0x1FFFFu; t5 = t5 < NENT ? t5 : 0u;
-            unsigned t6 = p6 & 0x1FFFFu; t6 = t6 < NENT ? t6 : 0u;
-            unsigned t7 = p7 & 0x1FFFFu; t7 = t7 < NENT ? t7 : 0u;
-            unsigned v0 = eA2[(long long)t0*64 + lane];
-            unsigned v1 = eA2[(long long)t1*64 + lane];
-            unsigned v2 = eA2[(long long)t2*64 + lane];
-            unsigned v3 = eA2[(long long)t3*64 + lane];
-            unsigned v4 = eA2[(long long)t4*64 + lane];
-            unsigned v5 = eA2[(long long)t5*64 + lane];
-            unsigned v6 = eA2[(long long)t6*64 + lane];
-            unsigned v7 = eA2[(long long)t7*64 + lane];
-            ac += pk_lo(v0)*wlc[((p0>>17)&15u)*64+lane] + pk_lo(v1)*wlc[((p1>>17)&15u)*64+lane]
-                + pk_lo(v2)*wlc[((p2>>17)&15u)*64+lane] + pk_lo(v3)*wlc[((p3>>17)&15u)*64+lane]
-                + pk_lo(v4)*wlc[((p4>>17)&15u)*64+lane] + pk_lo(v5)*wlc[((p5>>17)&15u)*64+lane]
-                + pk_lo(v6)*wlc[((p6>>17)&15u)*64+lane] + pk_lo(v7)*wlc[((p7>>17)&15u)*64+lane];
-            ad += pk_hi(v0)*wld[((p0>>21)&31u)*64+lane] + pk_hi(v1)*wld[((p1>>21)&31u)*64+lane]
-                + pk_hi(v2)*wld[((p2>>21)&31u)*64+lane] + pk_hi(v3)*wld[((p3>>21)&31u)*64+lane]
-                + pk_hi(v4)*wld[((p4>>21)&31u)*64+lane] + pk_hi(v5)*wld[((p5>>21)&31u)*64+lane]
-                + pk_hi(v6)*wld[((p6>>21)&31u)*64+lane] + pk_hi(v7)*wld[((p7>>21)&31u)*64+lane];
-        }
-        for (; k + 4 <= e_; k += 4){
-            unsigned p0 = rflu(epk[k]), p1 = rflu(epk[k+1]), p2 = rflu(epk[k+2]), p3 = rflu(epk[k+3]);
-            unsigned t0 = p0 & 0x1FFFFu; t0 = t0 < NENT ? t0 : 0u;
-            unsigned t1 = p1 & 0x1FFFFu; t1 = t1 < NENT ? t1 : 0u;
-            unsigned t2 = p2 & 0x1FFFFu; t2 = t2 < NENT ? t2 : 0u;
-            unsigned t3 = p3 & 0x1FFFFu; t3 = t3 < NENT ? t3 : 0u;
-            unsigned v0 = eA2[(long long)t0*64 + lane];
-            unsigned v1 = eA2[(long long)t1*64 + lane];
-            unsigned v2 = eA2[(long long)t2*64 + lane];
-            unsigned v3 = eA2[(long long)t3*64 + lane];
-            ac += pk_lo(v0)*wlc[((p0>>17)&15u)*64+lane] + pk_lo(v1)*wlc[((p1>>17)&15u)*64+lane]
-                + pk_lo(v2)*wlc[((p2>>17)&15u)*64+lane] + pk_lo(v3)*wlc[((p3>>17)&15u)*64+lane];
-            ad += pk_hi(v0)*wld[((p0>>21)&31u)*64+lane] + pk_hi(v1)*wld[((p1>>21)&31u)*64+lane]
-                + pk_hi(v2)*wld[((p2>>21)&31u)*64+lane] + pk_hi(v3)*wld[((p3>>21)&31u)*64+lane];
-        }
-        for (; k < e_; k++){
-            unsigned p = rflu(epk[k]);
-            unsigned ti = p & 0x1FFFFu; ti = ti < NENT ? ti : 0u;
-            unsigned v = eA2[(long long)ti*64 + lane];
-            ac += pk_lo(v) * wlc[((p>>17)&15u)*64+lane];
-            ad += pk_hi(v) * wld[((p>>21)&31u)*64+lane];
+        for (int kb = s; kb < e_; kb += 64){
+            int gi2 = kb + lane;
+            unsigned pkv = epk[gi2 < e_ ? gi2 : s];
+            int rem = e_ - kb; if (rem > 64) rem = 64;
+            int kk = 0;
+            for (; kk + 8 <= rem; kk += 8){
+                unsigned p0 = rdl(pkv, kk),   p1 = rdl(pkv, kk+1), p2 = rdl(pkv, kk+2), p3 = rdl(pkv, kk+3);
+                unsigned p4 = rdl(pkv, kk+4), p5 = rdl(pkv, kk+5), p6 = rdl(pkv, kk+6), p7 = rdl(pkv, kk+7);
+                unsigned t0 = p0 & 0x1FFFFu; t0 = t0 < NENT ? t0 : 0u;
+                unsigned t1 = p1 & 0x1FFFFu; t1 = t1 < NENT ? t1 : 0u;
+                unsigned t2 = p2 & 0x1FFFFu; t2 = t2 < NENT ? t2 : 0u;
+                unsigned t3 = p3 & 0x1FFFFu; t3 = t3 < NENT ? t3 : 0u;
+                unsigned t4 = p4 & 0x1FFFFu; t4 = t4 < NENT ? t4 : 0u;
+                unsigned t5 = p5 & 0x1FFFFu; t5 = t5 < NENT ? t5 : 0u;
+                unsigned t6 = p6 & 0x1FFFFu; t6 = t6 < NENT ? t6 : 0u;
+                unsigned t7 = p7 & 0x1FFFFu; t7 = t7 < NENT ? t7 : 0u;
+                unsigned v0 = eA2[(long long)t0*64 + lane];
+                unsigned v1 = eA2[(long long)t1*64 + lane];
+                unsigned v2 = eA2[(long long)t2*64 + lane];
+                unsigned v3 = eA2[(long long)t3*64 + lane];
+                unsigned v4 = eA2[(long long)t4*64 + lane];
+                unsigned v5 = eA2[(long long)t5*64 + lane];
+                unsigned v6 = eA2[(long long)t6*64 + lane];
+                unsigned v7 = eA2[(long long)t7*64 + lane];
+                ac += pk_lo(v0)*wlc[((p0>>17)&15u)*64+lane] + pk_lo(v1)*wlc[((p1>>17)&15u)*64+lane]
+                    + pk_lo(v2)*wlc[((p2>>17)&15u)*64+lane] + pk_lo(v3)*wlc[((p3>>17)&15u)*64+lane]
+                    + pk_lo(v4)*wlc[((p4>>17)&15u)*64+lane] + pk_lo(v5)*wlc[((p5>>17)&15u)*64+lane]
+                    + pk_lo(v6)*wlc[((p6>>17)&15u)*64+lane] + pk_lo(v7)*wlc[((p7>>17)&15u)*64+lane];
+                ad += pk_hi(v0)*wld[((p0>>21)&31u)*64+lane] + pk_hi(v1)*wld[((p1>>21)&31u)*64+lane]
+                    + pk_hi(v2)*wld[((p2>>21)&31u)*64+lane] + pk_hi(v3)*wld[((p3>>21)&31u)*64+lane]
+                    + pk_hi(v4)*wld[((p4>>21)&31u)*64+lane] + pk_hi(v5)*wld[((p5>>21)&31u)*64+lane]
+                    + pk_hi(v6)*wld[((p6>>21)&31u)*64+lane] + pk_hi(v7)*wld[((p7>>21)&31u)*64+lane];
+            }
+            for (; kk < rem; kk++){
+                unsigned p = rdl(pkv, kk);
+                unsigned ti = p & 0x1FFFFu; ti = ti < NENT ? ti : 0u;
+                unsigned v = eA2[(long long)ti*64 + lane];
+                ac += pk_lo(v) * wlc[((p>>17)&15u)*64+lane];
+                ad += pk_hi(v) * wld[((p>>21)&31u)*64+lane];
+            }
         }
         float inv_deg = 1.f / fmaxf((float)deg, 1.f);
         float vc = fin(ac) * inv_deg, vd = fin(ad) * inv_deg;
@@ -699,63 +691,51 @@
         int s = (int)(rd & 0xFFFFFu);
         int e_ = s + (int)(rd >> 20);
         float accc = 0.f, accd = 0.f;
-        int k = s;
-        for (; k + 8 <= e_; k += 8){
-            unsigned p0 = rflu(upk[k]),   p1 = rflu(upk[k+1]), p2 = rflu(upk[k+2]), p3 = rflu(upk[k+3]);
-            unsigned p4 = rflu(upk[k+4]), p5 = rflu(upk[k+5]), p6 = rflu(upk[k+6]), p7 = rflu(upk[k+7]);
-            unsigned c0 = p0 & 0x1FFFFu; c0 = c0 < NENT ? c0 : 0u;
-            unsigned c1 = p1 & 0x1FFFFu; c1 = c1 < NENT ? c1 : 0u;
-            unsigned c2 = p2 & 0x1FFFFu; c2 = c2 < NENT ? c2 : 0u;
-            unsigned c3 = p3 & 0x1FFFFu; c3 = c3 < NENT ? c3 : 0u;
-            unsigned c4 = p4 & 0x1FFFFu; c4 = c4 < NENT ? c4 : 0u;
-            unsigned c5 = p5 & 0x1FFFFu; c5 = c5 < NENT ? c5 : 0u;
-            unsigned c6 = p6 & 0x1FFFFu; c6 = c6 < NENT ? c6 : 0u;
-            unsigned c7 = p7 & 0x1FFFFu; c7 = c7 < NENT ? c7 : 0u;
-            unsigned g0 = eA2[(long long)c0*64 + lane];
-            unsigned g1 = eA2[(long long)c1*64 + lane];
-            unsigned g2 = eA2[(long long)c2*64 + lane];
-            unsigned g3 = eA2[(long long)c3*64 + lane];
-            unsigned g4 = eA2[(long long)c4*64 + lane];
-            unsigned g5 = eA2[(long long)c5*64 + lane];
-            unsigned g6 = eA2[(long long)c6*64 + lane];
-            unsigned g7 = eA2[(long long)c7*64 + lane];
-            float v0 = __uint_as_float(((p0 >> 17) & 0x7FFFu) << 16);
-            float v1 = __uint_as_float(((p1 >> 17) & 0x7FFFu) << 16);
-            float v2 = __uint_as_float(((p2 >> 17) & 0x7FFFu) << 16);
-            float v3 = __uint_as_float(((p3 >> 17) & 0x7FFFu) << 16);
-            float v4 = __uint_as_float(((p4 >> 17) & 0x7FFFu) << 16);
-            float v5 = __uint_as_float(((p5 >> 17) & 0x7FFFu) << 16);
-            float v6 = __uint_as_float(((p6 >> 17) & 0x7FFFu) << 16);
-            float v7 = __uint_as_float(((p7 >> 17) & 0x7FFFu) << 16);
-            accc += v0*pk_lo(g0) + v1*pk_lo(g1) + v2*pk_lo(g2) + v3*pk_lo(g3)
-                  + v4*pk_lo(g4) + v5*pk_lo(g5) + v6*pk_lo(g6) + v7*pk_lo(g7);
-            accd += v0*pk_hi(g0) + v1*pk_hi(g1) + v2*pk_hi(g2) + v3*pk_hi(g3)
-                  + v4*pk_hi(g4) + v5*pk_hi(g5) + v6*pk_hi(g6) + v7*pk_hi(g7);
-        }
-        for (; k + 4 <= e_; k += 4){
-            unsigned p0 = rflu(upk[k]), p1 = rflu(upk[k+1]), p2 = rflu(upk[k+2]), p3 = rflu(upk[k+3]);
-            unsigned c0 = p0 & 0x1FFFFu; c0 = c0 < NENT ? c0 : 0u;
-            unsigned c1 = p1 & 0x1FFFFu; c1 = c1 < NENT ? c1 : 0u;
-            unsigned c2 = p2 & 0x1FFFFu; c2 = c2 < NENT ? c2 : 0u;
-            unsigned c3 = p3 & 0x1FFFFu; c3 = c3 < NENT ? c3 : 0u;
-            float v0 = __uint_as_float(((p0 >> 17) & 0x7FFFu) << 16);
-            float v1 = __uint_as_float(((p1 >> 17) & 0x7FFFu) << 16);
-            float v2 = __uint_as_float(((p2 >> 17) & 0x7FFFu) << 16);
-            float v3 = __uint_as_float(((p3 >> 17) & 0x7FFFu) << 16);
-            unsigned g0 = eA2[(long long)c0*64 + lane];
-            unsigned g1 = eA2[(long long)c1*64 + lane];
-            unsigned g2 = eA2[(long long)c2*64 + lane];
-            unsigned g3 = eA2[(long long)c3*64 + lane];
-            accc += v0*pk_lo(g0) + v1*pk_lo(g1) + v2*pk_lo(g2) + v3*pk_lo(g3);
-            accd += v0*pk_hi(g0) + v1*pk_hi(g1) + v2*pk_hi(g2) + v3*pk_hi(g3);
-        }
-        for (; k < e_; k++){
-            unsigned p = rflu(upk[k]);
-            unsigned c = p & 0x1FFFFu; c = c < NENT ? c : 0u;
-            float v = __uint_as_float(((p >> 17) & 0x7FFFu) << 16);
-            unsigned g = eA2[(long long)c*64 + lane];
-            accc += v * pk_lo(g);
-            accd += v * pk_hi(g);
+        for (int kb = s; kb < e_; kb += 64){
+            int gi2 = kb + lane;
+            unsigned pkv = upk[gi2 < e_ ? gi2 : s];
+            int rem = e_ - kb; if (rem > 64) rem = 64;
+            int kk = 0;
+            for (; kk + 8 <= rem; kk += 8){
+                unsigned p0 = rdl(pkv, kk),   p1 = rdl(pkv, kk+1), p2 = rdl(pkv, kk+2), p3 = rdl(pkv, kk+3);
+                unsigned p4 = rdl(pkv, kk+4), p5 = rdl(pkv, kk+5), p6 = rdl(pkv, kk+6), p7 = rdl(pkv, kk+7);
+                unsigned c0 = p0 & 0x1FFFFu; c0 = c0 < NENT ? c0 : 0u;
+                unsigned c1 = p1 & 0x1FFFFu; c1 = c1 < NENT ? c1 : 0u;
+                unsigned c2 = p2 & 0x1FFFFu; c2 = c2 < NENT ? c2 : 0u;
+                unsigned c3 = p3 & 0x1FFFFu; c3 = c3 < NENT ? c3 : 0u;
+                unsigned c4 = p4 & 0x1FFFFu; c4 = c4 < NENT ? c4 : 0u;
+                unsigned c5 = p5 & 0x1FFFFu; c5 = c5 < NENT ? c5 : 0u;
+                unsigned c6 = p6 & 0x1FFFFu; c6 = c6 < NENT ? c6 : 0u;
+                unsigned c7 = p7 & 0x1FFFFu; c7 = c7 < NENT ? c7 : 0u;
+                unsigned g0 = eA2[(long long)c0*64 + lane];
+                unsigned g1 = eA2[(long long)c1*64 + lane];
+                unsigned g2 = eA2[(long long)c2*64 + lane];
+                unsigned g3 = eA2[(long long)c3*64 + lane];
+                unsigned g4 = eA2[(long long)c4*64 + lane];
+                unsigned g5 = eA2[(long long)c5*64 + lane];
+                unsigned g6 = eA2[(long long)c6*64 + lane];
+                unsigned g7 = eA2[(long long)c7*64 + lane];
+                float v0 = __uint_as_float(((p0 >> 17) & 0x7FFFu) << 16);
+                float v1 = __uint_as_float(((p1 >> 17) & 0x7FFFu) << 16);
+                float v2 = __uint_as_float(((p2 >> 17) & 0x7FFFu) << 16);
+                float v3 = __uint_as_float(((p3 >> 17) & 0x7FFFu) << 16);
+                float v4 = __uint_as_float(((p4 >> 17) & 0x7FFFu) << 16);
+                float v5 = __uint_as_float(((p5 >> 17) & 0x7FFFu) << 16);
+                float v6 = __uint_as_float(((p6 >> 17) & 0x7FFFu) << 16);
+                float v7 = __uint_as_float(((p7 >> 17) & 0x7FFFu) << 16);
+                accc += v0*pk_lo(g0) + v1*pk_lo(g1) + v2*pk_lo(g2) + v3*pk_lo(g3)
+                      + v4*pk_lo(g4) + v5*pk_lo(g5) + v6*pk_lo(g6) + v7*pk_lo(g7);
+                accd += v0*pk_hi(g0) + v1*pk_hi(g1) + v2*pk_hi(g2) + v3*pk_hi(g3)
+                      + v4*pk_hi(g4) + v5*pk_hi(g5) + v6*pk_hi(g6) + v7*pk_hi(g7);
+            }
+            for (; kk < rem; kk++){
+                unsigned p = rdl(pkv, kk);
+                unsigned c = p & 0x1FFFFu; c = c < NENT ? c : 0u;
+                float v = __uint_as_float(((p >> 17) & 0x7FFFu) << 16);
+                unsigned g = eA2[(long long)c*64 + lane];
+                accc += v * pk_lo(g);
+                accd += v * pk_hi(g);
+            }
         }
         long long ix = (long long)u*64 + lane;
         float xc = uc_io[ix], xd = ud_io[ix];
@@ -922,13 +902,14 @@
     float* oe_d = out + 9600001LL;
     float* ou_d = out + 16000001LL;
 
-    int gi = (NSH*NENT + 255)/256;
-    k_init<<<gi, 256, 0, stream>>>(deg8_e, deg8_u, ctrs);
-    if (tierA) k_conv<<<(NENT*CC+255)/256, 256, 0, stream>>>(entity_emb, ebf);
-    int gh = (EE + NNZI + 255)/256;
-    k_hist<<<gh, 256, 0, stream>>>(head, irows, deg8_e, deg8_u, rank_e, rank_u);
+    hipMemsetAsync(scratch_base, 0, 4915208, stream);
+    int convN = tierA ? (NENT*CC/4) : 0;
+    int gh = (EE + NNZI + convN + 255)/256;
+    k_hist<<<gh, 256, 0, stream>>>(head, irows, deg8_e, deg8_u, rank_e, rank_u,
+                                   entity_emb, tierA ? ebf : nullptr);
     k_base2<<<(NENT+255)/256, 256, 0, stream>>>(deg8_e, deg8_u, rsdeg_e, rsdeg_u, ctrs);
-    k_scatter<<<gh, 256, 0, stream>>>(head, tail, etype, cate, irows, icols, ivals,
+    int gs = (EE + NNZI + 255)/256;
+    k_scatter<<<gs, 256, 0, stream>>>(head, tail, etype, cate, irows, icols, ivals,
                                       rank_e, rank_u, deg8_e, deg8_u,
                                       rsdeg_e, rsdeg_u, epk, upk);
 
```

Result: slower. 830.3 us (+2.6%).
